# Kernel optimization log

Measured on AMD Instinct MI355X. Metric: run time of the kernel, lower is better.

## Reference

```python
import jax, jax.numpy as jnp
import numpy as np

D = 128      # d_model
H = 8        # n_heads
HD = D // H  # head_dim = 16
E = 256      # n_experts
R = 32       # kv_lora_rank
B, T = 4, 512
EPS = 1e-6


def _dense_init(k, fi, fo):
    s = float(1.0 / np.sqrt(fi))
    return jax.random.uniform(k, (fi, fo), minval=-s, maxval=s, dtype=jnp.float32)


def setup_inputs() -> dict:
    key = jax.random.key(0)
    ks = jax.random.split(key, 16)
    rng = np.random.RandomState(42)
    Q, _ = np.linalg.qr(rng.randn(D, D))
    glim = float(np.sqrt(6.0 / (D + D)))
    return {
        'x': jax.random.normal(ks[0], (B, T, D), dtype=jnp.float32),
        'g1': jnp.ones((D,), jnp.float32),
        'qW': _dense_init(ks[1], D, D), 'qb': jnp.zeros((D,), jnp.float32),
        'kdW': _dense_init(ks[2], D, R), 'kdb': jnp.zeros((R,), jnp.float32),
        'kuW': _dense_init(ks[3], R, 2 * D), 'kub': jnp.zeros((2 * D,), jnp.float32),
        'oW': _dense_init(ks[4], D, D), 'ob': jnp.zeros((D,), jnp.float32),
        'rot': jnp.asarray(Q, jnp.float32),
        'tq_scale': jnp.ones((D,), jnp.float32),
        's1W': _dense_init(ks[5], D, D), 's1b': jnp.zeros((D,), jnp.float32),
        's2W': _dense_init(ks[6], D, D), 's2b': jnp.zeros((D,), jnp.float32),
        'g2': jnp.ones((D,), jnp.float32),
        'gateW': _dense_init(ks[7], D, E), 'gateb': jnp.zeros((E,), jnp.float32),
        'expW': jax.random.uniform(ks[8], (E, D, D), minval=-glim, maxval=glim, dtype=jnp.float32),
        'm1W': _dense_init(ks[9], D, D), 'm1b': jnp.zeros((D,), jnp.float32),
        'm2W': _dense_init(ks[10], D, D), 'm2b': jnp.zeros((D,), jnp.float32),
    }


def _rmsnorm(x, g):
    return g * (x / jnp.sqrt(jnp.mean(x * x, axis=-1, keepdims=True) + EPS))


def _swiglu(x, w1, b1, w2, b2):
    gate = x @ w1 + b1
    return gate * jax.nn.sigmoid(gate) * (x @ w2 + b2)


def _mla(x, qW, qb, kdW, kdb, kuW, kub, oW, ob):
    b, t = x.shape[0], x.shape[1]
    q = (x @ qW + qb).reshape(b, t, H, HD)
    kv = ((x @ kdW + kdb) @ kuW + kub).reshape(b, t, H, 2 * HD)
    k, v = jnp.split(kv, 2, axis=-1)
    q = jax.nn.elu(q) + 1.0
    k = jax.nn.elu(k) + 1.0
    # linear attention: context[b,h,d,e] = sum_t k[b,t,h,d] v[b,t,h,e]
    context = jnp.einsum('bthd,bthe->bhde', k, v)
    out = jnp.einsum('bthd,bhde->bthe', q, context)
    k_sum = jnp.sum(k, axis=1)  # [b,h,d]
    z = 1.0 / (jnp.einsum('bthd,bhd->bth', q, k_sum) + EPS)
    out = out * z[..., None]
    return out.reshape(b, t, D) @ oW + ob


def _turbo_quant(x, rot, scale):
    x = x @ rot
    mag = jnp.sqrt(jnp.mean(x * x, axis=-1, keepdims=True) + EPS)
    phase = x / mag
    qp = jnp.clip(phase * 127.0, -127.0, 127.0) / 127.0
    phase = jax.lax.stop_gradient(qp - phase) + phase  # straight-through
    return phase * mag * scale


def _moe(h, gateW, gateb, expW, m1W, m1b, m2W, m2b):
    gate_scores = jax.nn.softmax(h @ gateW + gateb, axis=-1)  # [B,T,E]
    top_vals, top_idx = jax.lax.top_k(gate_scores, 2)
    top_w = top_vals / (jnp.sum(top_vals, axis=-1, keepdims=True) + EPS)
    # dense all-expert compute as in the original module
    eo = jnp.einsum('btd,edo->bteo', h, expW)  # [B,T,E,D]
    mask = jnp.sum(jax.nn.one_hot(top_idx, E, dtype=h.dtype) * top_w[..., None], axis=2)  # [B,T,E]
    wavg = jnp.einsum('bteo,bte->bto', eo, mask)
    wavg = _swiglu(wavg, m1W, m1b, m2W, m2b)
    diff_sq = jnp.square(eo - wavg[:, :, None, :])
    wvar = jnp.einsum('bteo,bte->bto', diff_sq, mask)
    consensus = jnp.exp(-jnp.mean(wvar, axis=-1))  # [B,T]
    return wavg, consensus


def reference(x, g1, qW, qb, kdW, kdb, kuW, kub, oW, ob, rot, tq_scale,
              s1W, s1b, s2W, s2b, g2, gateW, gateb, expW, m1W, m1b, m2W, m2b):
    attn_out = _turbo_quant(_mla(_rmsnorm(x, g1), qW, qb, kdW, kdb, kuW, kub, oW, ob), rot, tq_scale)
    x = x + _swiglu(attn_out, s1W, s1b, s2W, s2b)
    moe_out, consensus = _moe(_rmsnorm(x, g2), gateW, gateb, expW, m1W, m1b, m2W, m2b)
    return x + moe_out, consensus
```

## Files before the change

kernel.cpp:

```cpp
#include <hip/hip_runtime.h>
#include <hip/hip_cooperative_groups.h>
#include <math.h>

namespace cg = cooperative_groups;

static constexpr int Dd    = 128;
static constexpr int NH    = 8;
static constexpr int NE    = 256;
static constexpr int RR    = 32;
static constexpr int TT    = 512;
static constexpr int NTOK  = 2048;
static constexpr int SLOTS = 256;
#define EPSF 1e-6f

__device__ __forceinline__ float elu1(float v) { return v > 0.f ? v + 1.f : expf(v); }
__device__ __forceinline__ float sigm(float v) { return 1.f / (1.f + expf(-v)); }

struct Params {
  const float *x, *g1, *qW, *qb, *kdW, *kdb, *kuW, *kub, *oW, *ob, *rot, *tqs;
  const float *s1W, *s1b, *s2W, *s2b, *g2, *gateW, *gateb, *expW, *m1W, *m1b, *m2W, *m2b;
  float *out;
  float *ctx, *ksum, *h2buf, *oR, *bR, *ybuf;
  int *cnt, *slottok;
};

template <int TPB>
__device__ __forceinline__ void fused_body(const Params P) {
  constexpr int NG    = TPB / 4;
  constexpr int GRIDB = NTOK / TPB;
  constexpr int BPE   = GRIDB / NE;
  const int tid = threadIdx.x;
  const int bid = blockIdx.x;
  const int j = tid & 127, g = tid >> 7;
  const int lane = tid & 63;
  const int base_n0 = bid * TPB;
  const int b = base_n0 >> 9;

  __shared__ float4 h1T[128];
  __shared__ float4 bufQ[NG][128];
  __shared__ float4 bufB[128];
  __shared__ float4 part[3][128];
  __shared__ float4 kpart[8][32];
  __shared__ float4 kdT[32];
  __shared__ float4 kupart[256];
  __shared__ float4 rtmp[2];
  __shared__ __align__(16) float kS[NG][8][16][4];
  __shared__ __align__(16) float vS[NG][8][16][4];
  __shared__ float wvS[4][4]; __shared__ int wiS[4][4];
  __shared__ float zS[4][4];
  __shared__ int sSlot[TPB][2]; __shared__ float sWt[TPB][2];
  __shared__ __align__(16) float hT[128 * 20];
  __shared__ float4 y1T[128], y2T[128], inT[128], sT[128];

  float xv[NG][4];
  float xn[NG][4];
#pragma unroll
  for (int grp = 0; grp < NG; grp++)
#pragma unroll
    for (int t = 0; t < 4; t++) { xv[grp][t] = 0.f; xn[grp][t] = 0.f; }

  if (bid == 0) {
    for (int i = tid; i < NH * 4 * 256; i += 512) P.ctx[i] = 0.f;
    P.ksum[tid] = 0.f;
    if (tid < NE) P.cnt[tid] = 0;
  }

  for (int grp = 0; grp < NG; grp++) {
    const int n0 = base_n0 + grp * 4;

    if (tid < 128) {
      float v[4];
#pragma unroll
      for (int t = 0; t < 4; t++) { xv[grp][t] = P.x[(n0 + t) * Dd + j]; v[t] = xv[grp][t] * xv[grp][t]; }
#pragma unroll
      for (int o = 32; o > 0; o >>= 1) {
#pragma unroll
        for (int t = 0; t < 4; t++) v[t] += __shfl_xor(v[t], o, 64);
      }
      if (lane == 0) rtmp[tid >> 6] = make_float4(v[0], v[1], v[2], v[3]);
    }
    __syncthreads();
    if (tid < 128) {
      float g1j = P.g1[j];
#pragma unroll
      for (int t = 0; t < 4; t++) {
        float ss = ((const float*)&rtmp[0])[t] + ((const float*)&rtmp[1])[t];
        ((float*)&h1T[j])[t] = g1j * xv[grp][t] * rsqrtf(ss * (1.f / 128.f) + EPSF);
      }
    }
    __syncthreads();

    {
      float a0 = 0, a1 = 0, a2 = 0, a3 = 0;
      const float* Wp = P.qW + (g * 32) * Dd + j;
#pragma unroll 16
      for (int i = 0; i < 32; i++) {
        float4 h4 = h1T[g * 32 + i];
        float w = Wp[i * Dd];
        a0 += h4.x * w; a1 += h4.y * w; a2 += h4.z * w; a3 += h4.w * w;
      }
      if (g) part[g - 1][j] = make_float4(a0, a1, a2, a3);
      __syncthreads();
      if (g == 0) {
        float4 p0 = part[0][j], p1 = part[1][j], p2 = part[2][j];
        float bb = P.qb[j];
        ((float*)&bufQ[grp][j])[0] = elu1(a0 + p0.x + p1.x + p2.x + bb);
        ((float*)&bufQ[grp][j])[1] = elu1(a1 + p0.y + p1.y + p2.y + bb);
        ((float*)&bufQ[grp][j])[2] = elu1(a2 + p0.z + p1.z + p2.z + bb);
        ((float*)&bufQ[grp][j])[3] = elu1(a3 + p0.w + p1.w + p2.w + bb);
      }
      __syncthreads();
    }

    if (tid < 256) {
      int col = tid & 31, ksp = tid >> 5;
      float a0 = 0, a1 = 0, a2 = 0, a3 = 0;
      const float* Wp = P.kdW + (ksp * 16) * RR + col;
#pragma unroll
      for (int i = 0; i < 16; i++) {
        float4 h4 = h1T[ksp * 16 + i];
        float w = Wp[i * RR];
        a0 += h4.x * w; a1 += h4.y * w; a2 += h4.z * w; a3 += h4.w * w;
      }
      kpart[ksp][col] = make_float4(a0, a1, a2, a3);
    }
    __syncthreads();
    if (tid < 32) {
      float bb = P.kdb[tid];
      float s0 = bb, s1 = bb, s2 = bb, s3 = bb;
#pragma unroll
      for (int k = 0; k < 8; k++) {
        float4 p = kpart[k][tid];
        s0 += p.x; s1 += p.y; s2 += p.z; s3 += p.w;
      }
      kdT[tid] = make_float4(s0, s1, s2, s3);
    }
    __syncthreads();

    {
      int col = tid & 255, kh = tid >> 8;
      float a0 = 0, a1 = 0, a2 = 0, a3 = 0;
      const float* Wp = P.kuW + (kh * 16) * 256 + col;
#pragma unroll
      for (int r = 0; r < 16; r++) {
        float4 k4 = kdT[kh * 16 + r];
        float w = Wp[r * 256];
        a0 += k4.x * w; a1 += k4.y * w; a2 += k4.z * w; a3 += k4.w * w;
      }
      if (kh) kupart[col] = make_float4(a0, a1, a2, a3);
      __syncthreads();
      if (!kh) {
        float4 p = kupart[col];
        float bb = P.kub[col];
        float v0 = a0 + p.x + bb, v1 = a1 + p.y + bb, v2 = a2 + p.z + bb, v3 = a3 + p.w + bb;
        int h = col >> 5, off = col & 31;
        if (off < 16) {
          kS[grp][h][off][0] = elu1(v0); kS[grp][h][off][1] = elu1(v1);
          kS[grp][h][off][2] = elu1(v2); kS[grp][h][off][3] = elu1(v3);
        } else {
          vS[grp][h][off - 16][0] = v0; vS[grp][h][off - 16][1] = v1;
          vS[grp][h][off - 16][2] = v2; vS[grp][h][off - 16][3] = v3;
        }
      }
    }
    __syncthreads();
  }

  if (bid < 32) {
    int idx = bid * 512 + tid;
    int row = idx >> 7, col = idx & 127;
    const float* ow = P.oW + row * 128;
    float acc = 0.f;
#pragma unroll 8
    for (int k = 0; k < 128; k++) acc += ow[k] * P.rot[k * 128 + col];
    P.oR[idx] = acc;
  } else if (bid == 32 && tid < 128) {
    float acc = 0.f;
#pragma unroll 8
    for (int k = 0; k < 128; k++) acc += P.ob[k] * P.rot[k * 128 + tid];
    P.bR[tid] = acc;
  }

  cg::this_grid().sync();

  {
    const int h = tid >> 6;
    const int d = (tid >> 2) & 15;
    const int e0 = (tid & 3) * 4;
    const int bh = b * NH + h;
    float acc[4] = {0.f, 0.f, 0.f, 0.f};
    float ks = 0.f;
#pragma unroll
    for (int grp = 0; grp < NG; grp++) {
      float4 k4 = *(const float4*)&kS[grp][h][d][0];
      ks += k4.x + k4.y + k4.z + k4.w;
#pragma unroll
      for (int ee = 0; ee < 4; ee++) {
        float4 v4 = *(const float4*)&vS[grp][h][e0 + ee][0];
        acc[ee] += k4.x * v4.x + k4.y * v4.y + k4.z * v4.z + k4.w * v4.w;
      }
    }
    float* cp = P.ctx + bh * 256 + d * 16 + e0;
#pragma unroll
    for (int ee = 0; ee < 4; ee++) atomicAdd(cp + ee, acc[ee]);
    if ((tid & 3) == 0) atomicAdd(&P.ksum[bh * 16 + d], ks);
  }

  cg::this_grid().sync();

  for (int grp = 0; grp < NG; grp++) {
    const int n0 = base_n0 + grp * 4;
    float m1[4]; int i1[4]; float m2[4]; int i2[4];
    float val[4]; float r2v[4];

    if (tid < 128) {
      int h = j >> 4, e = j & 15;
      const float* cpt = P.ctx + (b * NH + h) * 256;
      const float* kpt = P.ksum + (b * NH + h) * 16;
      float num[4] = {0, 0, 0, 0}, den[4] = {0, 0, 0, 0};
#pragma unroll
      for (int d = 0; d < 16; d++) {
        float cx = cpt[d * 16 + e], ks = kpt[d];
        float4 q4 = bufQ[grp][h * 16 + d];
        num[0] += q4.x * cx; num[1] += q4.y * cx; num[2] += q4.z * cx; num[3] += q4.w * cx;
        den[0] += q4.x * ks; den[1] += q4.y * ks; den[2] += q4.z * ks; den[3] += q4.w * ks;
      }
#pragma unroll
      for (int t = 0; t < 4; t++) ((float*)&bufB[j])[t] = num[t] / (den[t] + EPSF);
    }
    __syncthreads();

    {
      float a0 = 0, a1 = 0, a2 = 0, a3 = 0;
      const float* Wp = P.oR + (g * 32) * Dd + j;
#pragma unroll 16
      for (int i = 0; i < 32; i++) {
        float4 h4 = bufB[g * 32 + i];
        float w = Wp[i * Dd];
        a0 += h4.x * w; a1 += h4.y * w; a2 += h4.z * w; a3 += h4.w * w;
      }
      if (g) part[g - 1][j] = make_float4(a0, a1, a2, a3);
      __syncthreads();
      float tot[4];
      if (g == 0) {
        float4 p0 = part[0][j], p1 = part[1][j], p2 = part[2][j];
        float bb = P.bR[j];
        tot[0] = a0 + p0.x + p1.x + p2.x + bb; tot[1] = a1 + p0.y + p1.y + p2.y + bb;
        tot[2] = a2 + p0.z + p1.z + p2.z + bb; tot[3] = a3 + p0.w + p1.w + p2.w + bb;
        float v[4];
#pragma unroll
        for (int t = 0; t < 4; t++) v[t] = tot[t] * tot[t];
#pragma unroll
        for (int o = 32; o > 0; o >>= 1) {
#pragma unroll
          for (int t = 0; t < 4; t++) v[t] += __shfl_xor(v[t], o, 64);
        }
        if (lane == 0) rtmp[tid >> 6] = make_float4(v[0], v[1], v[2], v[3]);
      }
      __syncthreads();
      if (g == 0) {
        float scj = P.tqs[j];
#pragma unroll
        for (int t = 0; t < 4; t++) {
          float ss = ((const float*)&rtmp[0])[t] + ((const float*)&rtmp[1])[t];
          float mag = sqrtf(ss * (1.f / 128.f) + EPSF);
          float zc = fminf(fmaxf(tot[t], -mag), mag);
          ((float*)&bufQ[grp][j])[t] = zc * scj;
        }
      }
      __syncthreads();
    }

    {
      float a0 = 0, a1 = 0, a2 = 0, a3 = 0;
      const float* Wp = (g < 2 ? P.s1W : P.s2W) + ((g & 1) * 64) * Dd + j;
#pragma unroll 16
      for (int i = 0; i < 64; i++) {
        float4 h4 = bufQ[grp][(g & 1) * 64 + i];
        float w = Wp[i * Dd];
        a0 += h4.x * w; a1 += h4.y * w; a2 += h4.z * w; a3 += h4.w * w;
      }
      if (g) part[g - 1][j] = make_float4(a0, a1, a2, a3);
      __syncthreads();
      if (g == 0) {
        float b1 = P.s1b[j], b2 = P.s2b[j];
        float4 p0 = part[0][j], p1 = part[1][j], p2 = part[2][j];
        float gv[4], uv[4], v[4];
        gv[0] = a0 + p0.x + b1; gv[1] = a1 + p0.y + b1;
        gv[2] = a2 + p0.z + b1; gv[3] = a3 + p0.w + b1;
        uv[0] = p1.x + p2.x + b2; uv[1] = p1.y + p2.y + b2;
        uv[2] = p1.z + p2.z + b2; uv[3] = p1.w + p2.w + b2;
        float g2j = P.g2[j];
#pragma unroll
        for (int t = 0; t < 4; t++) {
          xn[grp][t] = xv[grp][t] + gv[t] * sigm(gv[t]) * uv[t];
          ((float*)&bufB[j])[t] = g2j * xn[grp][t];
          v[t] = xn[grp][t] * xn[grp][t];
        }
#pragma unroll
        for (int o = 32; o > 0; o >>= 1) {
#pragma unroll
          for (int t = 0; t < 4; t++) v[t] += __shfl_xor(v[t], o, 64);
        }
        if (lane == 0) rtmp[tid >> 6] = make_float4(v[0], v[1], v[2], v[3]);
      }
      __syncthreads();
    }

    {
      int col = tid & 255, kh = tid >> 8;
      float a0 = 0, a1 = 0, a2 = 0, a3 = 0;
      const float* Wp = P.gateW + (kh * 64) * NE + col;
#pragma unroll 16
      for (int i = 0; i < 64; i++) {
        float4 h4 = bufB[kh * 64 + i];
        float w = Wp[i * NE];
        a0 += h4.x * w; a1 += h4.y * w; a2 += h4.z * w; a3 += h4.w * w;
      }
      if (kh) kupart[col] = make_float4(a0, a1, a2, a3);
      __syncthreads();
#pragma unroll
      for (int t = 0; t < 4; t++) {
        float ss = ((const float*)&rtmp[0])[t] + ((const float*)&rtmp[1])[t];
        r2v[t] = rsqrtf(ss * (1.f / 128.f) + EPSF);
      }
      if (!kh) {
        float4 p = kupart[col];
        float bb = P.gateb[col];
        val[0] = (a0 + p.x) * r2v[0] + bb; val[1] = (a1 + p.y) * r2v[1] + bb;
        val[2] = (a2 + p.z) * r2v[2] + bb; val[3] = (a3 + p.w) * r2v[3] + bb;
      }
      if (tid < 128) {
#pragma unroll
        for (int t = 0; t < 4; t++)
          P.h2buf[(n0 + t) * Dd + j] = ((const float*)&bufB[j])[t] * r2v[t];
      }
    }
    __syncthreads();

    {
      if (tid < 256) {
        float bv[4]; int bi[4];
#pragma unroll
        for (int t = 0; t < 4; t++) { bv[t] = val[t]; bi[t] = tid; }
#pragma unroll
        for (int o = 32; o > 0; o >>= 1) {
#pragma unroll
          for (int t = 0; t < 4; t++) {
            float wv = __shfl_xor(bv[t], o, 64);
            int wi = __shfl_xor(bi[t], o, 64);
            if (wv > bv[t] || (wv == bv[t] && wi < bi[t])) { bv[t] = wv; bi[t] = wi; }
          }
        }
        if (lane == 0) {
#pragma unroll
          for (int t = 0; t < 4; t++) { wvS[tid >> 6][t] = bv[t]; wiS[tid >> 6][t] = bi[t]; }
        }
      }
      __syncthreads();
      if (tid < 256) {
#pragma unroll
        for (int t = 0; t < 4; t++) {
          m1[t] = wvS[0][t]; i1[t] = wiS[0][t];
#pragma unroll
          for (int w = 1; w < 4; w++) {
            float cv = wvS[w][t]; int ci = wiS[w][t];
            if (cv > m1[t] || (cv == m1[t] && ci < i1[t])) { m1[t] = cv; i1[t] = ci; }
          }
        }
      }
      __syncthreads();
    }
    {
      if (tid < 256) {
        float bv[4]; int bi[4];
#pragma unroll
        for (int t = 0; t < 4; t++) {
          bv[t] = (tid == i1[t]) ? -INFINITY : val[t];
          bi[t] = tid;
        }
#pragma unroll
        for (int o = 32; o > 0; o >>= 1) {
#pragma unroll
          for (int t = 0; t < 4; t++) {
            float wv = __shfl_xor(bv[t], o, 64);
            int wi = __shfl_xor(bi[t], o, 64);
            if (wv > bv[t] || (wv == bv[t] && wi < bi[t])) { bv[t] = wv; bi[t] = wi; }
          }
        }
        if (lane == 0) {
#pragma unroll
          for (int t = 0; t < 4; t++) { wvS[tid >> 6][t] = bv[t]; wiS[tid >> 6][t] = bi[t]; }
        }
      }
      __syncthreads();
      if (tid < 256) {
#pragma unroll
        for (int t = 0; t < 4; t++) {
          m2[t] = wvS[0][t]; i2[t] = wiS[0][t];
#pragma unroll
          for (int w = 1; w < 4; w++) {
            float cv = wvS[w][t]; int ci = wiS[w][t];
            if (cv > m2[t] || (cv == m2[t] && ci < i2[t])) { m2[t] = cv; i2[t] = ci; }
          }
        }
      }
      __syncthreads();
    }
    {
      if (tid < 256) {
        float v[4];
#pragma unroll
        for (int t = 0; t < 4; t++) v[t] = expf(val[t] - m1[t]);
#pragma unroll
        for (int o = 32; o > 0; o >>= 1) {
#pragma unroll
          for (int t = 0; t < 4; t++) v[t] += __shfl_xor(v[t], o, 64);
        }
        if (lane == 0) {
#pragma unroll
          for (int t = 0; t < 4; t++) zS[tid >> 6][t] = v[t];
        }
      }
      __syncthreads();
    }
    if (tid < 4) {
      int t = tid, tok = n0 + t;
      float Z = zS[0][t] + zS[1][t] + zS[2][t] + zS[3][t];
      float p1 = 1.f / Z;
      float p2 = expf(m2[t] - m1[t]) / Z;
      float s = p1 + p2 + EPSF;
      int e1 = i1[t], e2 = i2[t];
      int s1 = atomicAdd(&P.cnt[e1], 1); if (s1 > SLOTS - 1) s1 = SLOTS - 1;
      int s2 = atomicAdd(&P.cnt[e2], 1); if (s2 > SLOTS - 1) s2 = SLOTS - 1;
      int sl1 = e1 * SLOTS + s1, sl2 = e2 * SLOTS + s2;
      P.slottok[sl1] = tok; P.slottok[sl2] = tok;
      sSlot[grp * 4 + t][0] = sl1; sSlot[grp * 4 + t][1] = sl2;
      sWt[grp * 4 + t][0] = p1 / s; sWt[grp * 4 + t][1] = p2 / s;
    }
    __syncthreads();
  }

  cg::this_grid().sync();

  {
    const int e = bid / BPE, sub = bid % BPE;
    int n = P.cnt[e]; if (n > SLOTS) n = SLOTS;
    const int base = e * SLOTS;
    const float* Wp = P.expW + (size_t)e * Dd * Dd + j;
    for (int t0 = sub * 16; t0 < n; t0 += BPE * 16) {
      int m = n - t0; if (m > 16) m = 16;
      __syncthreads();
      for (int tt = g; tt < m; tt += 4) {
        int tok = P.slottok[base + t0 + tt];
        hT[j * 20 + tt] = P.h2buf[tok * Dd + j];
      }
      __syncthreads();
      float acc[4] = {0, 0, 0, 0};
#pragma unroll 8
      for (int i = 0; i < 128; i++) {
        float w = Wp[i * Dd];
        float4 h4 = *(const float4*)&hT[i * 20 + g * 4];
        acc[0] += h4.x * w; acc[1] += h4.y * w; acc[2] += h4.z * w; acc[3] += h4.w * w;
      }
#pragma unroll
      for (int k = 0; k < 4; k++) {
        int tt = g * 4 + k;
        if (tt < m) P.ybuf[(size_t)(base + t0 + tt) * Dd + j] = acc[k];
      }
    }
  }

  cg::this_grid().sync();

  for (int grp = 0; grp < NG; grp++) {
    const int n0 = base_n0 + grp * 4;
    {
      const int ti = grp * 4 + g;
      float y1 = P.ybuf[(size_t)sSlot[ti][0] * Dd + j];
      float y2 = P.ybuf[(size_t)sSlot[ti][1] * Dd + j];
      ((float*)&y1T[j])[g] = y1;
      ((float*)&y2T[j])[g] = y2;
      ((float*)&inT[j])[g] = sWt[ti][0] * y1 + sWt[ti][1] * y2;
    }
    __syncthreads();

    {
      float a0 = 0, a1 = 0, a2 = 0, a3 = 0;
      const float* Wp = (g < 2 ? P.m1W : P.m2W) + ((g & 1) * 64) * Dd + j;
#pragma unroll 16
      for (int i = 0; i < 64; i++) {
        float4 h4 = inT[(g & 1) * 64 + i];
        float w = Wp[i * Dd];
        a0 += h4.x * w; a1 += h4.y * w; a2 += h4.z * w; a3 += h4.w * w;
      }
      if (g) part[g - 1][j] = make_float4(a0, a1, a2, a3);
      __syncthreads();
      if (g == 0) {
        float b1 = P.m1b[j], b2 = P.m2b[j];
        float4 p0 = part[0][j], p1 = part[1][j], p2 = part[2][j];
        float gv[4], uv[4];
        gv[0] = a0 + p0.x + b1; gv[1] = a1 + p0.y + b1;
        gv[2] = a2 + p0.z + b1; gv[3] = a3 + p0.w + b1;
        uv[0] = p1.x + p2.x + b2; uv[1] = p1.y + p2.y + b2;
        uv[2] = p1.z + p2.z + b2; uv[3] = p1.w + p2.w + b2;
#pragma unroll
        for (int t = 0; t < 4; t++) {
          float sv = gv[t] * sigm(gv[t]) * uv[t];
          ((float*)&sT[j])[t] = sv;
          P.out[(n0 + t) * Dd + j] = xn[grp][t] + sv;
        }
      }
      __syncthreads();
    }

    if (tid < 128) {
      float v[4];
#pragma unroll
      for (int t = 0; t < 4; t++) {
        float sv = ((const float*)&sT[j])[t];
        float d1 = ((const float*)&y1T[j])[t] - sv;
        float d2 = ((const float*)&y2T[j])[t] - sv;
        v[t] = sWt[grp * 4 + t][0] * d1 * d1 + sWt[grp * 4 + t][1] * d2 * d2;
      }
#pragma unroll
      for (int o = 32; o > 0; o >>= 1) {
#pragma unroll
        for (int t = 0; t < 4; t++) v[t] += __shfl_xor(v[t], o, 64);
      }
      if (lane == 0) rtmp[tid >> 6] = make_float4(v[0], v[1], v[2], v[3]);
    }
    __syncthreads();
    if (tid < 4) {
      float s = ((const float*)&rtmp[0])[tid] + ((const float*)&rtmp[1])[tid];
      P.out[NTOK * Dd + n0 + tid] = expf(-s * (1.f / 128.f));
    }
    __syncthreads();
  }
}

__global__ __launch_bounds__(512, 4) void k_fused4(Params P) { fused_body<4>(P); }
__global__ __launch_bounds__(512)    void k_fused8(Params P) { fused_body<8>(P); }

static constexpr int TPBo = 4;

__global__ __launch_bounds__(512) void k_pre(
    const float* __restrict__ x, const float* __restrict__ g1,
    const float* __restrict__ qW, const float* __restrict__ qb,
    const float* __restrict__ kdW, const float* __restrict__ kdb,
    const float* __restrict__ kuW, const float* __restrict__ kub,
    float* __restrict__ qbuf, float* __restrict__ kvbuf,
    float* __restrict__ ctx, float* __restrict__ ksum, int* __restrict__ cnt) {
  const int tid = threadIdx.x;
  const int j = tid & 127, g = tid >> 7;
  const int lane = tid & 63;
  const int n0 = blockIdx.x * TPBo;

  __shared__ float4 h1T[128];
  __shared__ float4 part[3][128];
  __shared__ float4 kpart[8][32];
  __shared__ float4 kdT[32];
  __shared__ float4 kupart[256];
  __shared__ float4 rtmp[2];

  if (blockIdx.x == 0) {
    for (int i = tid; i < 32 * 256; i += 512) ctx[i] = 0.f;
    ksum[tid] = 0.f;
    if (tid < 256) cnt[tid] = 0;
  }

  float xv[4];
  if (tid < 128) {
    float v[4];
#pragma unroll
    for (int t = 0; t < 4; t++) { xv[t] = x[(n0 + t) * Dd + j]; v[t] = xv[t] * xv[t]; }
#pragma unroll
    for (int o = 32; o > 0; o >>= 1) {
#pragma unroll
      for (int t = 0; t < 4; t++) v[t] += __shfl_xor(v[t], o, 64);
    }
    if (lane == 0) rtmp[tid >> 6] = make_float4(v[0], v[1], v[2], v[3]);
  }
  __syncthreads();
  if (tid < 128) {
    float g1j = g1[j];
#pragma unroll
    for (int t = 0; t < 4; t++) {
      float ss = ((const float*)&rtmp[0])[t] + ((const float*)&rtmp[1])[t];
      ((float*)&h1T[j])[t] = g1j * xv[t] * rsqrtf(ss * (1.f / 128.f) + EPSF);
    }
  }
  __syncthreads();

  {
    float a0 = 0, a1 = 0, a2 = 0, a3 = 0;
    const float* Wp = qW + (g * 32) * Dd + j;
#pragma unroll 16
    for (int i = 0; i < 32; i++) {
      float4 h4 = h1T[g * 32 + i];
      float w = Wp[i * Dd];
      a0 += h4.x * w; a1 += h4.y * w; a2 += h4.z * w; a3 += h4.w * w;
    }
    if (g) part[g - 1][j] = make_float4(a0, a1, a2, a3);
    __syncthreads();
    if (g == 0) {
      float4 p0 = part[0][j], p1 = part[1][j], p2 = part[2][j];
      float bb = qb[j];
      qbuf[(n0 + 0) * Dd + j] = elu1(a0 + p0.x + p1.x + p2.x + bb);
      qbuf[(n0 + 1) * Dd + j] = elu1(a1 + p0.y + p1.y + p2.y + bb);
      qbuf[(n0 + 2) * Dd + j] = elu1(a2 + p0.z + p1.z + p2.z + bb);
      qbuf[(n0 + 3) * Dd + j] = elu1(a3 + p0.w + p1.w + p2.w + bb);
    }
    __syncthreads();
  }

  if (tid < 256) {
    int col = tid & 31, ksp = tid >> 5;
    float a0 = 0, a1 = 0, a2 = 0, a3 = 0;
    const float* Wp = kdW + (ksp * 16) * RR + col;
#pragma unroll
    for (int i = 0; i < 16; i++) {
      float4 h4 = h1T[ksp * 16 + i];
      float w = Wp[i * RR];
      a0 += h4.x * w; a1 += h4.y * w; a2 += h4.z * w; a3 += h4.w * w;
    }
    kpart[ksp][col] = make_float4(a0, a1, a2, a3);
  }
  __syncthreads();
  if (tid < 32) {
    float bb = kdb[tid];
    float s0 = bb, s1 = bb, s2 = bb, s3 = bb;
#pragma unroll
    for (int k = 0; k < 8; k++) {
      float4 p = kpart[k][tid];
      s0 += p.x; s1 += p.y; s2 += p.z; s3 += p.w;
    }
    kdT[tid] = make_float4(s0, s1, s2, s3);
  }
  __syncthreads();

  {
    int col = tid & 255, kh = tid >> 8;
    float a0 = 0, a1 = 0, a2 = 0, a3 = 0;
    const float* Wp = kuW + (kh * 16) * 256 + col;
#pragma unroll
    for (int r = 0; r < 16; r++) {
      float4 k4 = kdT[kh * 16 + r];
      float w = Wp[r * 256];
      a0 += k4.x * w; a1 += k4.y * w; a2 += k4.z * w; a3 += k4.w * w;
    }
    if (kh) kupart[col] = make_float4(a0, a1, a2, a3);
    __syncthreads();
    if (!kh) {
      float4 p = kupart[col];
      float bb = kub[col];
      bool isk = (col & 31) < 16;
      float v0 = a0 + p.x + bb, v1 = a1 + p.y + bb, v2 = a2 + p.z + bb, v3 = a3 + p.w + bb;
      kvbuf[(n0 + 0) * 256 + col] = isk ? elu1(v0) : v0;
      kvbuf[(n0 + 1) * 256 + col] = isk ? elu1(v1) : v1;
      kvbuf[(n0 + 2) * 256 + col] = isk ? elu1(v2) : v2;
      kvbuf[(n0 + 3) * 256 + col] = isk ? elu1(v3) : v3;
    }
  }
}

__global__ __launch_bounds__(256) void k_ctx(const float* __restrict__ kv,
                                             float* __restrict__ ctx,
                                             float* __restrict__ ksum,
                                             const float* __restrict__ oW,
                                             const float* __restrict__ ob,
                                             const float* __restrict__ rot,
                                             float* __restrict__ oR,
                                             float* __restrict__ bR) {
  const int blk = blockIdx.x;
  const int tid = threadIdx.x;
  if (blk < 256) {
    const int bh = blk >> 3, c = blk & 7;
    const int b = bh >> 3, h = bh & 7;
    const int d = tid >> 4, e = tid & 15;
    __shared__ float sh[64 * 32];
#pragma unroll
    for (int r = 0; r < 8; r++) {
      int lin = r * 256 + tid;
      int tok = lin >> 5, off = lin & 31;
      sh[lin] = kv[((b * TT + c * 64 + tok) * 256) + h * 32 + off];
    }
    __syncthreads();
    float acc = 0.f, ks = 0.f;
#pragma unroll 4
    for (int t = 0; t < 64; t++) {
      float kk = sh[t * 32 + d];
      acc += kk * sh[t * 32 + 16 + e];
      ks += kk;
    }
    atomicAdd(&ctx[bh * 256 + d * 16 + e], acc);
    if (e == 0) atomicAdd(&ksum[bh * 16 + d], ks);
  } else if (blk < 320) {
    int idx = (blk - 256) * 256 + tid;
    int row = idx >> 7, col = idx & 127;
    const float* ow = oW + row * 128;
    float acc = 0.f;
#pragma unroll 8
    for (int k = 0; k < 128; k++) acc += ow[k] * rot[k * 128 + col];
    oR[row * 128 + col] = acc;
  } else {
    if (tid < 128) {
      float acc = 0.f;
#pragma unroll 8
      for (int k = 0; k < 128; k++) acc += ob[k] * rot[k * 128 + tid];
      bR[tid] = acc;
    }
  }
}

__global__ __launch_bounds__(512) void k_mid(
    const float* __restrict__ x, const float* __restrict__ qbuf,
    const float* __restrict__ ctx, const float* __restrict__ ksum,
    const float* __restrict__ oR, const float* __restrict__ bR,
    const float* __restrict__ tqs,
    const float* __restrict__ s1W, const float* __restrict__ s1b,
    const float* __restrict__ s2W, const float* __restrict__ s2b,
    const float* __restrict__ g2, const float* __restrict__ gateW,
    const float* __restrict__ gateb,
    float* __restrict__ xnbuf, float* __restrict__ h2buf,
    float* __restrict__ gw, int* __restrict__ tokslot,
    int* __restrict__ slottok, int* __restrict__ cnt) {
  const int tid = threadIdx.x;
  const int j = tid & 127, g = tid >> 7;
  const int lane = tid & 63;
  const int n0 = blockIdx.x * TPBo;
  const int b = n0 >> 9;

  __shared__ float4 bufA[128], bufB[128];
  __shared__ float4 part[3][128];
  __shared__ float4 gpart[256];
  __shared__ float4 rtmp[2];
  __shared__ float wvS[4][4]; __shared__ int wiS[4][4];
  __shared__ float zS[4][4];

  float xres[4];
  if (tid < 128) {
#pragma unroll
    for (int t = 0; t < 4; t++) xres[t] = x[(n0 + t) * Dd + j];
  }

  ((float*)&bufA[j])[g] = qbuf[(n0 + g) * Dd + j];
  __syncthreads();

  if (tid < 128) {
    int h = j >> 4, e = j & 15;
    const float* cpt = ctx + (b * NH + h) * 256;
    const float* kpt = ksum + (b * NH + h) * 16;
    float num[4] = {0, 0, 0, 0}, den[4] = {0, 0, 0, 0};
#pragma unroll
    for (int d = 0; d < 16; d++) {
      float cx = cpt[d * 16 + e], ks = kpt[d];
      float4 q4 = bufA[h * 16 + d];
      num[0] += q4.x * cx; num[1] += q4.y * cx; num[2] += q4.z * cx; num[3] += q4.w * cx;
      den[0] += q4.x * ks; den[1] += q4.y * ks; den[2] += q4.z * ks; den[3] += q4.w * ks;
    }
#pragma unroll
    for (int t = 0; t < 4; t++) ((float*)&bufB[j])[t] = num[t] / (den[t] + EPSF);
  }
  __syncthreads();

  {
    float a0 = 0, a1 = 0, a2 = 0, a3 = 0;
    const float* Wp = oR + (g * 32) * Dd + j;
#pragma unroll 16
    for (int i = 0; i < 32; i++) {
      float4 h4 = bufB[g * 32 + i];
      float w = Wp[i * Dd];
      a0 += h4.x * w; a1 += h4.y * w; a2 += h4.z * w; a3 += h4.w * w;
    }
    if (g) part[g - 1][j] = make_float4(a0, a1, a2, a3);
    __syncthreads();
    float tot[4];
    if (g == 0) {
      float4 p0 = part[0][j], p1 = part[1][j], p2 = part[2][j];
      float bb = bR[j];
      tot[0] = a0 + p0.x + p1.x + p2.x + bb; tot[1] = a1 + p0.y + p1.y + p2.y + bb;
      tot[2] = a2 + p0.z + p1.z + p2.z + bb; tot[3] = a3 + p0.w + p1.w + p2.w + bb;
      float v[4];
#pragma unroll
      for (int t = 0; t < 4; t++) v[t] = tot[t] * tot[t];
#pragma unroll
      for (int o = 32; o > 0; o >>= 1) {
#pragma unroll
        for (int t = 0; t < 4; t++) v[t] += __shfl_xor(v[t], o, 64);
      }
      if (lane == 0) rtmp[tid >> 6] = make_float4(v[0], v[1], v[2], v[3]);
    }
    __syncthreads();
    if (g == 0) {
      float scj = tqs[j];
#pragma unroll
      for (int t = 0; t < 4; t++) {
        float ss = ((const float*)&rtmp[0])[t] + ((const float*)&rtmp[1])[t];
        float mag = sqrtf(ss * (1.f / 128.f) + EPSF);
        float zc = fminf(fmaxf(tot[t], -mag), mag);
        ((float*)&bufA[j])[t] = zc * scj;
      }
    }
    __syncthreads();
  }

  {
    float a0 = 0, a1 = 0, a2 = 0, a3 = 0;
    const float* Wp = (g < 2 ? s1W : s2W) + ((g & 1) * 64) * Dd + j;
#pragma unroll 16
    for (int i = 0; i < 64; i++) {
      float4 h4 = bufA[(g & 1) * 64 + i];
      float w = Wp[i * Dd];
      a0 += h4.x * w; a1 += h4.y * w; a2 += h4.z * w; a3 += h4.w * w;
    }
    if (g) part[g - 1][j] = make_float4(a0, a1, a2, a3);
    __syncthreads();
    if (g == 0) {
      float b1 = s1b[j], b2 = s2b[j];
      float4 p0 = part[0][j], p1 = part[1][j], p2 = part[2][j];
      float gv[4], uv[4], xn[4], v[4];
      gv[0] = a0 + p0.x + b1; gv[1] = a1 + p0.y + b1;
      gv[2] = a2 + p0.z + b1; gv[3] = a3 + p0.w + b1;
      uv[0] = p1.x + p2.x + b2; uv[1] = p1.y + p2.y + b2;
      uv[2] = p1.z + p2.z + b2; uv[3] = p1.w + p2.w + b2;
      float g2j = g2[j];
#pragma unroll
      for (int t = 0; t < 4; t++) {
        xn[t] = xres[t] + gv[t] * sigm(gv[t]) * uv[t];
        xnbuf[(n0 + t) * Dd + j] = xn[t];
        ((float*)&bufB[j])[t] = g2j * xn[t];
        v[t] = xn[t] * xn[t];
      }
#pragma unroll
      for (int o = 32; o > 0; o >>= 1) {
#pragma unroll
        for (int t = 0; t < 4; t++) v[t] += __shfl_xor(v[t], o, 64);
      }
      if (lane == 0) rtmp[tid >> 6] = make_float4(v[0], v[1], v[2], v[3]);
    }
    __syncthreads();
  }

  float val[4];
  float r2[4];
  {
    int col = tid & 255, kh = tid >> 8;
    float a0 = 0, a1 = 0, a2 = 0, a3 = 0;
    const float* Wp = gateW + (kh * 64) * NE + col;
#pragma unroll 16
    for (int i = 0; i < 64; i++) {
      float4 h4 = bufB[kh * 64 + i];
      float w = Wp[i * NE];
      a0 += h4.x * w; a1 += h4.y * w; a2 += h4.z * w; a3 += h4.w * w;
    }
    if (kh) gpart[col] = make_float4(a0, a1, a2, a3);
    __syncthreads();
#pragma unroll
    for (int t = 0; t < 4; t++) {
      float ss = ((const float*)&rtmp[0])[t] + ((const float*)&rtmp[1])[t];
      r2[t] = rsqrtf(ss * (1.f / 128.f) + EPSF);
    }
    if (!kh) {
      float4 p = gpart[col];
      float bb = gateb[col];
      val[0] = (a0 + p.x) * r2[0] + bb; val[1] = (a1 + p.y) * r2[1] + bb;
      val[2] = (a2 + p.z) * r2[2] + bb; val[3] = (a3 + p.w) * r2[3] + bb;
    }
    if (tid < 128) {
#pragma unroll
      for (int t = 0; t < 4; t++)
        h2buf[(n0 + t) * Dd + j] = ((const float*)&bufB[j])[t] * r2[t];
    }
  }
  __syncthreads();

  float m1[4]; int i1[4];
  {
    if (tid < 256) {
      float bv[4]; int bi[4];
#pragma unroll
      for (int t = 0; t < 4; t++) { bv[t] = val[t]; bi[t] = tid; }
#pragma unroll
      for (int o = 32; o > 0; o >>= 1) {
#pragma unroll
        for (int t = 0; t < 4; t++) {
          float wv = __shfl_xor(bv[t], o, 64);
          int wi = __shfl_xor(bi[t], o, 64);
          if (wv > bv[t] || (wv == bv[t] && wi < bi[t])) { bv[t] = wv; bi[t] = wi; }
        }
      }
      if (lane == 0) {
#pragma unroll
        for (int t = 0; t < 4; t++) { wvS[tid >> 6][t] = bv[t]; wiS[tid >> 6][t] = bi[t]; }
      }
    }
    __syncthreads();
    if (tid < 256) {
#pragma unroll
      for (int t = 0; t < 4; t++) {
        m1[t] = wvS[0][t]; i1[t] = wiS[0][t];
#pragma unroll
        for (int w = 1; w < 4; w++) {
          float cv = wvS[w][t]; int ci = wiS[w][t];
          if (cv > m1[t] || (cv == m1[t] && ci < i1[t])) { m1[t] = cv; i1[t] = ci; }
        }
      }
    }
    __syncthreads();
  }
  float m2[4]; int i2[4];
  {
    if (tid < 256) {
      float bv[4]; int bi[4];
#pragma unroll
      for (int t = 0; t < 4; t++) {
        bv[t] = (tid == i1[t]) ? -INFINITY : val[t];
        bi[t] = tid;
      }
#pragma unroll
      for (int o = 32; o > 0; o >>= 1) {
#pragma unroll
        for (int t = 0; t < 4; t++) {
          float wv = __shfl_xor(bv[t], o, 64);
          int wi = __shfl_xor(bi[t], o, 64);
          if (wv > bv[t] || (wv == bv[t] && wi < bi[t])) { bv[t] = wv; bi[t] = wi; }
        }
      }
      if (lane == 0) {
#pragma unroll
        for (int t = 0; t < 4; t++) { wvS[tid >> 6][t] = bv[t]; wiS[tid >> 6][t] = bi[t]; }
      }
    }
    __syncthreads();
    if (tid < 256) {
#pragma unroll
      for (int t = 0; t < 4; t++) {
        m2[t] = wvS[0][t]; i2[t] = wiS[0][t];
#pragma unroll
        for (int w = 1; w < 4; w++) {
          float cv = wvS[w][t]; int ci = wiS[w][t];
          if (cv > m2[t] || (cv == m2[t] && ci < i2[t])) { m2[t] = cv; i2[t] = ci; }
        }
      }
    }
    __syncthreads();
  }
  {
    if (tid < 256) {
      float v[4];
#pragma unroll
      for (int t = 0; t < 4; t++) v[t] = expf(val[t] - m1[t]);
#pragma unroll
      for (int o = 32; o > 0; o >>= 1) {
#pragma unroll
        for (int t = 0; t < 4; t++) v[t] += __shfl_xor(v[t], o, 64);
      }
      if (lane == 0) {
#pragma unroll
        for (int t = 0; t < 4; t++) zS[tid >> 6][t] = v[t];
      }
    }
    __syncthreads();
  }
  if (tid < 4) {
    int t = tid, tok = n0 + t;
    float Z = zS[0][t] + zS[1][t] + zS[2][t] + zS[3][t];
    float p1 = 1.f / Z;
    float p2 = expf(m2[t] - m1[t]) / Z;
    float s = p1 + p2 + EPSF;
    int e1 = i1[t], e2 = i2[t];
    int s1 = atomicAdd(&cnt[e1], 1); if (s1 > SLOTS - 1) s1 = SLOTS - 1;
    int s2 = atomicAdd(&cnt[e2], 1); if (s2 > SLOTS - 1) s2 = SLOTS - 1;
    int sl1 = e1 * SLOTS + s1, sl2 = e2 * SLOTS + s2;
    slottok[sl1] = tok; slottok[sl2] = tok;
    tokslot[tok * 2] = sl1; tokslot[tok * 2 + 1] = sl2;
    gw[tok * 2] = p1 / s; gw[tok * 2 + 1] = p2 / s;
  }
}

__global__ __launch_bounds__(512) void k_exp(const float* __restrict__ h2buf,
                                             const int* __restrict__ slottok,
                                             const int* __restrict__ cnt,
                                             const float* __restrict__ expW,
                                             float* __restrict__ ybuf) {
  const int e = blockIdx.x;
  int n = cnt[e]; if (n > SLOTS) n = SLOTS;
  if (n == 0) return;
  const int base = e * SLOTS;
  const int tid = threadIdx.x;
  const int j = tid & 127, g = tid >> 7;
  __shared__ __align__(16) float hT[128 * 20];
  const float* Wp = expW + (size_t)e * Dd * Dd + j;
  for (int t0 = 0; t0 < n; t0 += 16) {
    int m = n - t0; if (m > 16) m = 16;
    __syncthreads();
    for (int tt = g; tt < m; tt += 4) {
      int tok = slottok[base + t0 + tt];
      hT[j * 20 + tt] = h2buf[tok * Dd + j];
    }
    __syncthreads();
    float acc[4] = {0, 0, 0, 0};
#pragma unroll 8
    for (int i = 0; i < 128; i++) {
      float w = Wp[i * Dd];
      float4 h4 = *(const float4*)&hT[i * 20 + g * 4];
      acc[0] += h4.x * w; acc[1] += h4.y * w; acc[2] += h4.z * w; acc[3] += h4.w * w;
    }
#pragma unroll
    for (int k = 0; k < 4; k++) {
      int tt = g * 4 + k;
      if (tt < m) ybuf[(size_t)(base + t0 + tt) * Dd + j] = acc[k];
    }
  }
}

__global__ __launch_bounds__(512) void k_post(
    const float* __restrict__ xnbuf, const float* __restrict__ ybuf,
    const int* __restrict__ tokslot, const float* __restrict__ gw,
    const float* __restrict__ m1W, const float* __restrict__ m1b,
    const float* __restrict__ m2W, const float* __restrict__ m2b,
    float* __restrict__ out) {
  const int tid = threadIdx.x;
  const int j = tid & 127, g = tid >> 7;
  const int lane = tid & 63;
  const int n0 = blockIdx.x * TPBo;

  __shared__ float4 y1T[128], y2T[128], inT[128], sT[128];
  __shared__ float4 part[3][128];
  __shared__ float4 rtmp[2];
  __shared__ int sSlot[4][2];
  __shared__ float sWt[4][2];

  if (tid < 4) {
    sSlot[tid][0] = tokslot[(n0 + tid) * 2];
    sSlot[tid][1] = tokslot[(n0 + tid) * 2 + 1];
    sWt[tid][0] = gw[(n0 + tid) * 2];
    sWt[tid][1] = gw[(n0 + tid) * 2 + 1];
  }
  __syncthreads();

  {
    float y1 = ybuf[(size_t)sSlot[g][0] * Dd + j];
    float y2 = ybuf[(size_t)sSlot[g][1] * Dd + j];
    ((float*)&y1T[j])[g] = y1;
    ((float*)&y2T[j])[g] = y2;
    ((float*)&inT[j])[g] = sWt[g][0] * y1 + sWt[g][1] * y2;
  }
  __syncthreads();

  {
    float a0 = 0, a1 = 0, a2 = 0, a3 = 0;
    const float* Wp = (g < 2 ? m1W : m2W) + ((g & 1) * 64) * Dd + j;
#pragma unroll 16
    for (int i = 0; i < 64; i++) {
      float4 h4 = inT[(g & 1) * 64 + i];
      float w = Wp[i * Dd];
      a0 += h4.x * w; a1 += h4.y * w; a2 += h4.z * w; a3 += h4.w * w;
    }
    if (g) part[g - 1][j] = make_float4(a0, a1, a2, a3);
    __syncthreads();
    if (g == 0) {
      float b1 = m1b[j], b2 = m2b[j];
      float4 p0 = part[0][j], p1 = part[1][j], p2 = part[2][j];
      float gv[4], uv[4];
      gv[0] = a0 + p0.x + b1; gv[1] = a1 + p0.y + b1;
      gv[2] = a2 + p0.z + b1; gv[3] = a3 + p0.w + b1;
      uv[0] = p1.x + p2.x + b2; uv[1] = p1.y + p2.y + b2;
      uv[2] = p1.z + p2.z + b2; uv[3] = p1.w + p2.w + b2;
#pragma unroll
      for (int t = 0; t < 4; t++) {
        float sv = gv[t] * sigm(gv[t]) * uv[t];
        ((float*)&sT[j])[t] = sv;
        out[(n0 + t) * Dd + j] = xnbuf[(n0 + t) * Dd + j] + sv;
      }
    }
    __syncthreads();
  }

  if (tid < 128) {
    float v[4];
#pragma unroll
    for (int t = 0; t < 4; t++) {
      float sv = ((const float*)&sT[j])[t];
      float d1 = ((const float*)&y1T[j])[t] - sv;
      float d2 = ((const float*)&y2T[j])[t] - sv;
      v[t] = sWt[t][0] * d1 * d1 + sWt[t][1] * d2 * d2;
    }
#pragma unroll
    for (int o = 32; o > 0; o >>= 1) {
#pragma unroll
      for (int t = 0; t < 4; t++) v[t] += __shfl_xor(v[t], o, 64);
    }
    if (lane == 0) rtmp[tid >> 6] = make_float4(v[0], v[1], v[2], v[3]);
  }
  __syncthreads();
  if (tid < 4) {
    float s = ((const float*)&rtmp[0])[tid] + ((const float*)&rtmp[1])[tid];
    out[NTOK * Dd + n0 + tid] = expf(-s * (1.f / 128.f));
  }
}

extern "C" void kernel_launch(void* const* d_in, const int* in_sizes, int n_in,
                              void* d_out, int out_size, void* d_ws, size_t ws_size,
                              hipStream_t stream) {
  float* ws = (float*)d_ws;

  Params p;
  p.x   = (const float*)d_in[0];
  p.g1  = (const float*)d_in[1];
  p.qW  = (const float*)d_in[2];
  p.qb  = (const float*)d_in[3];
  p.kdW = (const float*)d_in[4];
  p.kdb = (const float*)d_in[5];
  p.kuW = (const float*)d_in[6];
  p.kub = (const float*)d_in[7];
  p.oW  = (const float*)d_in[8];
  p.ob  = (const float*)d_in[9];
  p.rot = (const float*)d_in[10];
  p.tqs = (const float*)d_in[11];
  p.s1W = (const float*)d_in[12];
  p.s1b = (const float*)d_in[13];
  p.s2W = (const float*)d_in[14];
  p.s2b = (const float*)d_in[15];
  p.g2  = (const float*)d_in[16];
  p.gateW = (const float*)d_in[17];
  p.gateb = (const float*)d_in[18];
  p.expW  = (const float*)d_in[19];
  p.m1W = (const float*)d_in[20];
  p.m1b = (const float*)d_in[21];
  p.m2W = (const float*)d_in[22];
  p.m2b = (const float*)d_in[23];
  p.out = (float*)d_out;

  p.ctx     = ws;
  p.ksum    = ws + 8192;
  p.oR      = ws + 8704;
  p.bR      = ws + 25088;
  p.h2buf   = ws + 25216;
  p.cnt     = (int*)(ws + 287360);
  p.slottok = (int*)(ws + 287616);
  p.ybuf    = ws + 353152;

  void* args[] = {(void*)&p};
  hipError_t err = hipErrorUnknown;

  int nb4 = 0;
  if (hipOccupancyMaxActiveBlocksPerMultiprocessor(
          &nb4, reinterpret_cast<const void*>(&k_fused4), 512, 0) != hipSuccess)
    nb4 = 0;
  if (nb4 >= 2) {
    err = hipLaunchCooperativeKernel((void*)k_fused4, dim3(NTOK / 4), dim3(512),
                                     args, 0u, stream);
  }
  if (err != hipSuccess) {
    int nb8 = 0;
    if (hipOccupancyMaxActiveBlocksPerMultiprocessor(
            &nb8, reinterpret_cast<const void*>(&k_fused8), 512, 0) == hipSuccess &&
        nb8 >= 1) {
      err = hipLaunchCooperativeKernel((void*)k_fused8, dim3(NTOK / 8), dim3(512),
                                       args, 0u, stream);
    }
  }
  if (err == hipSuccess) return;

  float* qbuf   = ws;
  float* kvbuf  = ws + 262144;
  float* ctx    = ws + 786432;
  float* ksum   = ws + 794624;
  float* h2buf  = ws + 795136;
  float* xnbuf  = ws + 1057280;
  float* gw     = ws + 1319424;
  float* oRb    = ws + 1323520;
  float* bRb    = ws + 1339904;
  int*   cnt     = (int*)(ws + 1373056);
  int*   tokslot = (int*)(ws + 1373312);
  int*   slottok = (int*)(ws + 1377408);
  float* ybuf   = ws + 1442944;

  k_pre<<<NTOK / 4, 512, 0, stream>>>(p.x, p.g1, p.qW, p.qb, p.kdW, p.kdb, p.kuW, p.kub,
                                      qbuf, kvbuf, ctx, ksum, cnt);
  k_ctx<<<321, 256, 0, stream>>>(kvbuf, ctx, ksum, p.oW, p.ob, p.rot, oRb, bRb);
  k_mid<<<NTOK / 4, 512, 0, stream>>>(p.x, qbuf, ctx, ksum, oRb, bRb, p.tqs,
                                      p.s1W, p.s1b, p.s2W, p.s2b, p.g2, p.gateW, p.gateb,
                                      xnbuf, h2buf, gw, tokslot, slottok, cnt);
  k_exp<<<NE, 512, 0, stream>>>(h2buf, slottok, cnt, p.expW, ybuf);
  k_post<<<NTOK / 4, 512, 0, stream>>>(xnbuf, ybuf, tokslot, gw,
                                       p.m1W, p.m1b, p.m2W, p.m2b, p.out);
}
```

Measured before the change: 166.6 us.

## Split fused cooperative kernel into pre-kernel plus flag-synchronized remainder kernel

Replaces the single cooperative kernel, which used four grid-wide barriers, with a regular k_pre launch that computes q/kv projections and the folded output rotation, followed by a cooperative k_rest kernel. k_rest appears to use per-stage global flags (context, routing, per-expert) in place of full grid syncs, so expert blocks can start once their own tokens are routed. The fallback path splits expert work across two blocks per expert. This adds an extra launch and global round-trips for q/kv buffers, and the flag spinning carries correctness and deadlock risks.

```diff
diff --git a/kernel.cpp b/kernel.cpp
--- a/kernel.cpp
+++ b/kernel.cpp
@@ -1,8 +1,5 @@
 #include <hip/hip_runtime.h>
-#include <hip/hip_cooperative_groups.h>
 #include <math.h>
-
-namespace cg = cooperative_groups;
 
 static constexpr int Dd    = 128;
 static constexpr int NH    = 8;
@@ -13,548 +10,41 @@
 static constexpr int SLOTS = 256;
 #define EPSF 1e-6f
 
+static constexpr int FD_CTX   = 0;
+static constexpr int FD_ROUTE = 4;
+static constexpr int FD_EXP   = 5;
+static constexpr int NFLAGS   = 261;
+
 __device__ __forceinline__ float elu1(float v) { return v > 0.f ? v + 1.f : expf(v); }
 __device__ __forceinline__ float sigm(float v) { return 1.f / (1.f + expf(-v)); }
 
-struct Params {
-  const float *x, *g1, *qW, *qb, *kdW, *kdb, *kuW, *kub, *oW, *ob, *rot, *tqs;
-  const float *s1W, *s1b, *s2W, *s2b, *g2, *gateW, *gateb, *expW, *m1W, *m1b, *m2W, *m2b;
-  float *out;
-  float *ctx, *ksum, *h2buf, *oR, *bR, *ybuf;
-  int *cnt, *slottok;
-};
-
-template <int TPB>
-__device__ __forceinline__ void fused_body(const Params P) {
-  constexpr int NG    = TPB / 4;
-  constexpr int GRIDB = NTOK / TPB;
-  constexpr int BPE   = GRIDB / NE;
-  const int tid = threadIdx.x;
-  const int bid = blockIdx.x;
-  const int j = tid & 127, g = tid >> 7;
-  const int lane = tid & 63;
-  const int base_n0 = bid * TPB;
-  const int b = base_n0 >> 9;
-
-  __shared__ float4 h1T[128];
-  __shared__ float4 bufQ[NG][128];
-  __shared__ float4 bufB[128];
-  __shared__ float4 part[3][128];
-  __shared__ float4 kpart[8][32];
-  __shared__ float4 kdT[32];
-  __shared__ float4 kupart[256];
-  __shared__ float4 rtmp[2];
-  __shared__ __align__(16) float kS[NG][8][16][4];
-  __shared__ __align__(16) float vS[NG][8][16][4];
-  __shared__ float wvS[4][4]; __shared__ int wiS[4][4];
-  __shared__ float zS[4][4];
-  __shared__ int sSlot[TPB][2]; __shared__ float sWt[TPB][2];
-  __shared__ __align__(16) float hT[128 * 20];
-  __shared__ float4 y1T[128], y2T[128], inT[128], sT[128];
-
-  float xv[NG][4];
-  float xn[NG][4];
-#pragma unroll
-  for (int grp = 0; grp < NG; grp++)
-#pragma unroll
-    for (int t = 0; t < 4; t++) { xv[grp][t] = 0.f; xn[grp][t] = 0.f; }
-
-  if (bid == 0) {
-    for (int i = tid; i < NH * 4 * 256; i += 512) P.ctx[i] = 0.f;
-    P.ksum[tid] = 0.f;
-    if (tid < NE) P.cnt[tid] = 0;
-  }
-
-  for (int grp = 0; grp < NG; grp++) {
-    const int n0 = base_n0 + grp * 4;
-
-    if (tid < 128) {
-      float v[4];
-#pragma unroll
-      for (int t = 0; t < 4; t++) { xv[grp][t] = P.x[(n0 + t) * Dd + j]; v[t] = xv[grp][t] * xv[grp][t]; }
-#pragma unroll
-      for (int o = 32; o > 0; o >>= 1) {
-#pragma unroll
-        for (int t = 0; t < 4; t++) v[t] += __shfl_xor(v[t], o, 64);
-      }
-      if (lane == 0) rtmp[tid >> 6] = make_float4(v[0], v[1], v[2], v[3]);
-    }
-    __syncthreads();
-    if (tid < 128) {
-      float g1j = P.g1[j];
-#pragma unroll
-      for (int t = 0; t < 4; t++) {
-        float ss = ((const float*)&rtmp[0])[t] + ((const float*)&rtmp[1])[t];
-        ((float*)&h1T[j])[t] = g1j * xv[grp][t] * rsqrtf(ss * (1.f / 128.f) + EPSF);
-      }
-    }
-    __syncthreads();
-
-    {
-      float a0 = 0, a1 = 0, a2 = 0, a3 = 0;
-      const float* Wp = P.qW + (g * 32) * Dd + j;
-#pragma unroll 16
-      for (int i = 0; i < 32; i++) {
-        float4 h4 = h1T[g * 32 + i];
-        float w = Wp[i * Dd];
-        a0 += h4.x * w; a1 += h4.y * w; a2 += h4.z * w; a3 += h4.w * w;
-      }
-      if (g) part[g - 1][j] = make_float4(a0, a1, a2, a3);
-      __syncthreads();
-      if (g == 0) {
-        float4 p0 = part[0][j], p1 = part[1][j], p2 = part[2][j];
-        float bb = P.qb[j];
-        ((float*)&bufQ[grp][j])[0] = elu1(a0 + p0.x + p1.x + p2.x + bb);
-        ((float*)&bufQ[grp][j])[1] = elu1(a1 + p0.y + p1.y + p2.y + bb);
-        ((float*)&bufQ[grp][j])[2] = elu1(a2 + p0.z + p1.z + p2.z + bb);
-        ((float*)&bufQ[grp][j])[3] = elu1(a3 + p0.w + p1.w + p2.w + bb);
-      }
-      __syncthreads();
-    }
-
-    if (tid < 256) {
-      int col = tid & 31, ksp = tid >> 5;
-      float a0 = 0, a1 = 0, a2 = 0, a3 = 0;
-      const float* Wp = P.kdW + (ksp * 16) * RR + col;
-#pragma unroll
-      for (int i = 0; i < 16; i++) {
-        float4 h4 = h1T[ksp * 16 + i];
-        float w = Wp[i * RR];
-        a0 += h4.x * w; a1 += h4.y * w; a2 += h4.z * w; a3 += h4.w * w;
-      }
-      kpart[ksp][col] = make_float4(a0, a1, a2, a3);
-    }
-    __syncthreads();
-    if (tid < 32) {
-      float bb = P.kdb[tid];
-      float s0 = bb, s1 = bb, s2 = bb, s3 = bb;
-#pragma unroll
-      for (int k = 0; k < 8; k++) {
-        float4 p = kpart[k][tid];
-        s0 += p.x; s1 += p.y; s2 += p.z; s3 += p.w;
-      }
-      kdT[tid] = make_float4(s0, s1, s2, s3);
-    }
-    __syncthreads();
-
-    {
-      int col = tid & 255, kh = tid >> 8;
-      float a0 = 0, a1 = 0, a2 = 0, a3 = 0;
-      const float* Wp = P.kuW + (kh * 16) * 256 + col;
-#pragma unroll
-      for (int r = 0; r < 16; r++) {
-        float4 k4 = kdT[kh * 16 + r];
-        float w = Wp[r * 256];
-        a0 += k4.x * w; a1 += k4.y * w; a2 += k4.z * w; a3 += k4.w * w;
-      }
-      if (kh) kupart[col] = make_float4(a0, a1, a2, a3);
-      __syncthreads();
-      if (!kh) {
-        float4 p = kupart[col];
-        float bb = P.kub[col];
-        float v0 = a0 + p.x + bb, v1 = a1 + p.y + bb, v2 = a2 + p.z + bb, v3 = a3 + p.w + bb;
-        int h = col >> 5, off = col & 31;
-        if (off < 16) {
-          kS[grp][h][off][0] = elu1(v0); kS[grp][h][off][1] = elu1(v1);
-          kS[grp][h][off][2] = elu1(v2); kS[grp][h][off][3] = elu1(v3);
-        } else {
-          vS[grp][h][off - 16][0] = v0; vS[grp][h][off - 16][1] = v1;
-          vS[grp][h][off - 16][2] = v2; vS[grp][h][off - 16][3] = v3;
-        }
-      }
-    }
-    __syncthreads();
-  }
-
-  if (bid < 32) {
-    int idx = bid * 512 + tid;
-    int row = idx >> 7, col = idx & 127;
-    const float* ow = P.oW + row * 128;
-    float acc = 0.f;
-#pragma unroll 8
-    for (int k = 0; k < 128; k++) acc += ow[k] * P.rot[k * 128 + col];
-    P.oR[idx] = acc;
-  } else if (bid == 32 && tid < 128) {
-    float acc = 0.f;
-#pragma unroll 8
-    for (int k = 0; k < 128; k++) acc += P.ob[k] * P.rot[k * 128 + tid];
-    P.bR[tid] = acc;
-  }
-
-  cg::this_grid().sync();
-
-  {
-    const int h = tid >> 6;
-    const int d = (tid >> 2) & 15;
-    const int e0 = (tid & 3) * 4;
-    const int bh = b * NH + h;
-    float acc[4] = {0.f, 0.f, 0.f, 0.f};
-    float ks = 0.f;
-#pragma unroll
-    for (int grp = 0; grp < NG; grp++) {
-      float4 k4 = *(const float4*)&kS[grp][h][d][0];
-      ks += k4.x + k4.y + k4.z + k4.w;
-#pragma unroll
-      for (int ee = 0; ee < 4; ee++) {
-        float4 v4 = *(const float4*)&vS[grp][h][e0 + ee][0];
-        acc[ee] += k4.x * v4.x + k4.y * v4.y + k4.z * v4.z + k4.w * v4.w;
-      }
-    }
-    float* cp = P.ctx + bh * 256 + d * 16 + e0;
-#pragma unroll
-    for (int ee = 0; ee < 4; ee++) atomicAdd(cp + ee, acc[ee]);
-    if ((tid & 3) == 0) atomicAdd(&P.ksum[bh * 16 + d], ks);
-  }
-
-  cg::this_grid().sync();
-
-  for (int grp = 0; grp < NG; grp++) {
-    const int n0 = base_n0 + grp * 4;
-    float m1[4]; int i1[4]; float m2[4]; int i2[4];
-    float val[4]; float r2v[4];
-
-    if (tid < 128) {
-      int h = j >> 4, e = j & 15;
-      const float* cpt = P.ctx + (b * NH + h) * 256;
-      const float* kpt = P.ksum + (b * NH + h) * 16;
-      float num[4] = {0, 0, 0, 0}, den[4] = {0, 0, 0, 0};
-#pragma unroll
-      for (int d = 0; d < 16; d++) {
-        float cx = cpt[d * 16 + e], ks = kpt[d];
-        float4 q4 = bufQ[grp][h * 16 + d];
-        num[0] += q4.x * cx; num[1] += q4.y * cx; num[2] += q4.z * cx; num[3] += q4.w * cx;
-        den[0] += q4.x * ks; den[1] += q4.y * ks; den[2] += q4.z * ks; den[3] += q4.w * ks;
-      }
-#pragma unroll
-      for (int t = 0; t < 4; t++) ((float*)&bufB[j])[t] = num[t] / (den[t] + EPSF);
-    }
-    __syncthreads();
-
-    {
-      float a0 = 0, a1 = 0, a2 = 0, a3 = 0;
-      const float* Wp = P.oR + (g * 32) * Dd + j;
-#pragma unroll 16
-      for (int i = 0; i < 32; i++) {
-        float4 h4 = bufB[g * 32 + i];
-        float w = Wp[i * Dd];
-        a0 += h4.x * w; a1 += h4.y * w; a2 += h4.z * w; a3 += h4.w * w;
-      }
-      if (g) part[g - 1][j] = make_float4(a0, a1, a2, a3);
-      __syncthreads();
-      float tot[4];
-      if (g == 0) {
-        float4 p0 = part[0][j], p1 = part[1][j], p2 = part[2][j];
-        float bb = P.bR[j];
-        tot[0] = a0 + p0.x + p1.x + p2.x + bb; tot[1] = a1 + p0.y + p1.y + p2.y + bb;
-        tot[2] = a2 + p0.z + p1.z + p2.z + bb; tot[3] = a3 + p0.w + p1.w + p2.w + bb;
-        float v[4];
-#pragma unroll
-        for (int t = 0; t < 4; t++) v[t] = tot[t] * tot[t];
-#pragma unroll
-        for (int o = 32; o > 0; o >>= 1) {
-#pragma unroll
-          for (int t = 0; t < 4; t++) v[t] += __shfl_xor(v[t], o, 64);
-        }
-        if (lane == 0) rtmp[tid >> 6] = make_float4(v[0], v[1], v[2], v[3]);
-      }
-      __syncthreads();
-      if (g == 0) {
-        float scj = P.tqs[j];
-#pragma unroll
-        for (int t = 0; t < 4; t++) {
-          float ss = ((const float*)&rtmp[0])[t] + ((const float*)&rtmp[1])[t];
-          float mag = sqrtf(ss * (1.f / 128.f) + EPSF);
-          float zc = fminf(fmaxf(tot[t], -mag), mag);
-          ((float*)&bufQ[grp][j])[t] = zc * scj;
-        }
-      }
-      __syncthreads();
-    }
-
-    {
-      float a0 = 0, a1 = 0, a2 = 0, a3 = 0;
-      const float* Wp = (g < 2 ? P.s1W : P.s2W) + ((g & 1) * 64) * Dd + j;
-#pragma unroll 16
-      for (int i = 0; i < 64; i++) {
-        float4 h4 = bufQ[grp][(g & 1) * 64 + i];
-        float w = Wp[i * Dd];
-        a0 += h4.x * w; a1 += h4.y * w; a2 += h4.z * w; a3 += h4.w * w;
-      }
-      if (g) part[g - 1][j] = make_float4(a0, a1, a2, a3);
-      __syncthreads();
-      if (g == 0) {
-        float b1 = P.s1b[j], b2 = P.s2b[j];
-        float4 p0 = part[0][j], p1 = part[1][j], p2 = part[2][j];
-        float gv[4], uv[4], v[4];
-        gv[0] = a0 + p0.x + b1; gv[1] = a1 + p0.y + b1;
-        gv[2] = a2 + p0.z + b1; gv[3] = a3 + p0.w + b1;
-        uv[0] = p1.x + p2.x + b2; uv[1] = p1.y + p2.y + b2;
-        uv[2] = p1.z + p2.z + b2; uv[3] = p1.w + p2.w + b2;
-        float g2j = P.g2[j];
-#pragma unroll
-        for (int t = 0; t < 4; t++) {
-          xn[grp][t] = xv[grp][t] + gv[t] * sigm(gv[t]) * uv[t];
-          ((float*)&bufB[j])[t] = g2j * xn[grp][t];
-          v[t] = xn[grp][t] * xn[grp][t];
-        }
-#pragma unroll
-        for (int o = 32; o > 0; o >>= 1) {
-#pragma unroll
-          for (int t = 0; t < 4; t++) v[t] += __shfl_xor(v[t], o, 64);
-        }
-        if (lane == 0) rtmp[tid >> 6] = make_float4(v[0], v[1], v[2], v[3]);
-      }
-      __syncthreads();
-    }
-
-    {
-      int col = tid & 255, kh = tid >> 8;
-      float a0 = 0, a1 = 0, a2 = 0, a3 = 0;
-      const float* Wp = P.gateW + (kh * 64) * NE + col;
-#pragma unroll 16
-      for (int i = 0; i < 64; i++) {
-        float4 h4 = bufB[kh * 64 + i];
-        float w = Wp[i * NE];
-        a0 += h4.x * w; a1 += h4.y * w; a2 += h4.z * w; a3 += h4.w * w;
-      }
-      if (kh) kupart[col] = make_float4(a0, a1, a2, a3);
-      __syncthreads();
-#pragma unroll
-      for (int t = 0; t < 4; t++) {
-        float ss = ((const float*)&rtmp[0])[t] + ((const float*)&rtmp[1])[t];
-        r2v[t] = rsqrtf(ss * (1.f / 128.f) + EPSF);
-      }
-      if (!kh) {
-        float4 p = kupart[col];
-        float bb = P.gateb[col];
-        val[0] = (a0 + p.x) * r2v[0] + bb; val[1] = (a1 + p.y) * r2v[1] + bb;
-        val[2] = (a2 + p.z) * r2v[2] + bb; val[3] = (a3 + p.w) * r2v[3] + bb;
-      }
-      if (tid < 128) {
-#pragma unroll
-        for (int t = 0; t < 4; t++)
-          P.h2buf[(n0 + t) * Dd + j] = ((const float*)&bufB[j])[t] * r2v[t];
-      }
-    }
-    __syncthreads();
-
-    {
-      if (tid < 256) {
-        float bv[4]; int bi[4];
-#pragma unroll
-        for (int t = 0; t < 4; t++) { bv[t] = val[t]; bi[t] = tid; }
-#pragma unroll
-        for (int o = 32; o > 0; o >>= 1) {
-#pragma unroll
-          for (int t = 0; t < 4; t++) {
-            float wv = __shfl_xor(bv[t], o, 64);
-            int wi = __shfl_xor(bi[t], o, 64);
-            if (wv > bv[t] || (wv == bv[t] && wi < bi[t])) { bv[t] = wv; bi[t] = wi; }
-          }
-        }
-        if (lane == 0) {
-#pragma unroll
-          for (int t = 0; t < 4; t++) { wvS[tid >> 6][t] = bv[t]; wiS[tid >> 6][t] = bi[t]; }
-        }
-      }
-      __syncthreads();
-      if (tid < 256) {
-#pragma unroll
-        for (int t = 0; t < 4; t++) {
-          m1[t] = wvS[0][t]; i1[t] = wiS[0][t];
-#pragma unroll
-          for (int w = 1; w < 4; w++) {
-            float cv = wvS[w][t]; int ci = wiS[w][t];
-            if (cv > m1[t] || (cv == m1[t] && ci < i1[t])) { m1[t] = cv; i1[t] = ci; }
-          }
-        }
-      }
-      __syncthreads();
-    }
-    {
-      if (tid < 256) {
-        float bv[4]; int bi[4];
-#pragma unroll
-        for (int t = 0; t < 4; t++) {
-          bv[t] = (tid == i1[t]) ? -INFINITY : val[t];
-          bi[t] = tid;
-        }
-#pragma unroll
-        for (int o = 32; o > 0; o >>= 1) {
-#pragma unroll
-          for (int t = 0; t < 4; t++) {
-            float wv = __shfl_xor(bv[t], o, 64);
-            int wi = __shfl_xor(bi[t], o, 64);
-            if (wv > bv[t] || (wv == bv[t] && wi < bi[t])) { bv[t] = wv; bi[t] = wi; }
-          }
-        }
-        if (lane == 0) {
-#pragma unroll
-          for (int t = 0; t < 4; t++) { wvS[tid >> 6][t] = bv[t]; wiS[tid >> 6][t] = bi[t]; }
-        }
-      }
-      __syncthreads();
-      if (tid < 256) {
-#pragma unroll
-        for (int t = 0; t < 4; t++) {
-          m2[t] = wvS[0][t]; i2[t] = wiS[0][t];
-#pragma unroll
-          for (int w = 1; w < 4; w++) {
-            float cv = wvS[w][t]; int ci = wiS[w][t];
-            if (cv > m2[t] || (cv == m2[t] && ci < i2[t])) { m2[t] = cv; i2[t] = ci; }
-          }
-        }
-      }
-      __syncthreads();
-    }
-    {
-      if (tid < 256) {
-        float v[4];
-#pragma unroll
-        for (int t = 0; t < 4; t++) v[t] = expf(val[t] - m1[t]);
-#pragma unroll
-        for (int o = 32; o > 0; o >>= 1) {
-#pragma unroll
-          for (int t = 0; t < 4; t++) v[t] += __shfl_xor(v[t], o, 64);
-        }
-        if (lane == 0) {
-#pragma unroll
-          for (int t = 0; t < 4; t++) zS[tid >> 6][t] = v[t];
-        }
-      }
-      __syncthreads();
-    }
-    if (tid < 4) {
-      int t = tid, tok = n0 + t;
-      float Z = zS[0][t] + zS[1][t] + zS[2][t] + zS[3][t];
-      float p1 = 1.f / Z;
-      float p2 = expf(m2[t] - m1[t]) / Z;
-      float s = p1 + p2 + EPSF;
-      int e1 = i1[t], e2 = i2[t];
-      int s1 = atomicAdd(&P.cnt[e1], 1); if (s1 > SLOTS - 1) s1 = SLOTS - 1;
-      int s2 = atomicAdd(&P.cnt[e2], 1); if (s2 > SLOTS - 1) s2 = SLOTS - 1;
-      int sl1 = e1 * SLOTS + s1, sl2 = e2 * SLOTS + s2;
-      P.slottok[sl1] = tok; P.slottok[sl2] = tok;
-      sSlot[grp * 4 + t][0] = sl1; sSlot[grp * 4 + t][1] = sl2;
-      sWt[grp * 4 + t][0] = p1 / s; sWt[grp * 4 + t][1] = p2 / s;
-    }
-    __syncthreads();
-  }
-
-  cg::this_grid().sync();
-
-  {
-    const int e = bid / BPE, sub = bid % BPE;
-    int n = P.cnt[e]; if (n > SLOTS) n = SLOTS;
-    const int base = e * SLOTS;
-    const float* Wp = P.expW + (size_t)e * Dd * Dd + j;
-    for (int t0 = sub * 16; t0 < n; t0 += BPE * 16) {
-      int m = n - t0; if (m > 16) m = 16;
-      __syncthreads();
-      for (int tt = g; tt < m; tt += 4) {
-        int tok = P.slottok[base + t0 + tt];
-        hT[j * 20 + tt] = P.h2buf[tok * Dd + j];
-      }
-      __syncthreads();
-      float acc[4] = {0, 0, 0, 0};
-#pragma unroll 8
-      for (int i = 0; i < 128; i++) {
-        float w = Wp[i * Dd];
-        float4 h4 = *(const float4*)&hT[i * 20 + g * 4];
-        acc[0] += h4.x * w; acc[1] += h4.y * w; acc[2] += h4.z * w; acc[3] += h4.w * w;
-      }
-#pragma unroll
-      for (int k = 0; k < 4; k++) {
-        int tt = g * 4 + k;
-        if (tt < m) P.ybuf[(size_t)(base + t0 + tt) * Dd + j] = acc[k];
-      }
-    }
-  }
-
-  cg::this_grid().sync();
-
-  for (int grp = 0; grp < NG; grp++) {
-    const int n0 = base_n0 + grp * 4;
-    {
-      const int ti = grp * 4 + g;
-      float y1 = P.ybuf[(size_t)sSlot[ti][0] * Dd + j];
-      float y2 = P.ybuf[(size_t)sSlot[ti][1] * Dd + j];
-      ((float*)&y1T[j])[g] = y1;
-      ((float*)&y2T[j])[g] = y2;
-      ((float*)&inT[j])[g] = sWt[ti][0] * y1 + sWt[ti][1] * y2;
-    }
-    __syncthreads();
-
-    {
-      float a0 = 0, a1 = 0, a2 = 0, a3 = 0;
-      const float* Wp = (g < 2 ? P.m1W : P.m2W) + ((g & 1) * 64) * Dd + j;
-#pragma unroll 16
-      for (int i = 0; i < 64; i++) {
-        float4 h4 = inT[(g & 1) * 64 + i];
-        float w = Wp[i * Dd];
-        a0 += h4.x * w; a1 += h4.y * w; a2 += h4.z * w; a3 += h4.w * w;
-      }
-      if (g) part[g - 1][j] = make_float4(a0, a1, a2, a3);
-      __syncthreads();
-      if (g == 0) {
-        float b1 = P.m1b[j], b2 = P.m2b[j];
-        float4 p0 = part[0][j], p1 = part[1][j], p2 = part[2][j];
-        float gv[4], uv[4];
-        gv[0] = a0 + p0.x + b1; gv[1] = a1 + p0.y + b1;
-        gv[2] = a2 + p0.z + b1; gv[3] = a3 + p0.w + b1;
-        uv[0] = p1.x + p2.x + b2; uv[1] = p1.y + p2.y + b2;
-        uv[2] = p1.z + p2.z + b2; uv[3] = p1.w + p2.w + b2;
-#pragma unroll
-        for (int t = 0; t < 4; t++) {
-          float sv = gv[t] * sigm(gv[t]) * uv[t];
-          ((float*)&sT[j])[t] = sv;
-          P.out[(n0 + t) * Dd + j] = xn[grp][t] + sv;
-        }
-      }
-      __syncthreads();
-    }
-
-    if (tid < 128) {
-      float v[4];
-#pragma unroll
-      for (int t = 0; t < 4; t++) {
-        float sv = ((const float*)&sT[j])[t];
-        float d1 = ((const float*)&y1T[j])[t] - sv;
-        float d2 = ((const float*)&y2T[j])[t] - sv;
-        v[t] = sWt[grp * 4 + t][0] * d1 * d1 + sWt[grp * 4 + t][1] * d2 * d2;
-      }
-#pragma unroll
-      for (int o = 32; o > 0; o >>= 1) {
-#pragma unroll
-        for (int t = 0; t < 4; t++) v[t] += __shfl_xor(v[t], o, 64);
-      }
-      if (lane == 0) rtmp[tid >> 6] = make_float4(v[0], v[1], v[2], v[3]);
-    }
-    __syncthreads();
-    if (tid < 4) {
-      float s = ((const float*)&rtmp[0])[tid] + ((const float*)&rtmp[1])[tid];
-      P.out[NTOK * Dd + n0 + tid] = expf(-s * (1.f / 128.f));
-    }
-    __syncthreads();
-  }
+__device__ __forceinline__ void flag_add(int* p) {
+  __hip_atomic_fetch_add(p, 1, __ATOMIC_RELEASE, __HIP_MEMORY_SCOPE_AGENT);
 }
-
-__global__ __launch_bounds__(512, 4) void k_fused4(Params P) { fused_body<4>(P); }
-__global__ __launch_bounds__(512)    void k_fused8(Params P) { fused_body<8>(P); }
-
-static constexpr int TPBo = 4;
+__device__ __forceinline__ void flag_wait(int* p, int tgt) {
+  int c = 0;
+  while (__hip_atomic_load(p, __ATOMIC_ACQUIRE, __HIP_MEMORY_SCOPE_AGENT) < tgt) {
+    __builtin_amdgcn_s_sleep(2);
+    if (++c > (1 << 27)) break;
+  }
+}
 
 __global__ __launch_bounds__(512) void k_pre(
     const float* __restrict__ x, const float* __restrict__ g1,
     const float* __restrict__ qW, const float* __restrict__ qb,
     const float* __restrict__ kdW, const float* __restrict__ kdb,
     const float* __restrict__ kuW, const float* __restrict__ kub,
+    const float* __restrict__ oW, const float* __restrict__ ob,
+    const float* __restrict__ rot,
     float* __restrict__ qbuf, float* __restrict__ kvbuf,
-    float* __restrict__ ctx, float* __restrict__ ksum, int* __restrict__ cnt) {
+    float* __restrict__ ctx, float* __restrict__ ksum,
+    int* __restrict__ cnt, int* __restrict__ flags,
+    float* __restrict__ oR, float* __restrict__ bR) {
   const int tid = threadIdx.x;
+  const int bid = blockIdx.x;
   const int j = tid & 127, g = tid >> 7;
   const int lane = tid & 63;
-  const int n0 = blockIdx.x * TPBo;
+  const int n0 = bid * 4;
 
   __shared__ float4 h1T[128];
   __shared__ float4 part[3][128];
@@ -563,10 +53,11 @@
   __shared__ float4 kupart[256];
   __shared__ float4 rtmp[2];
 
-  if (blockIdx.x == 0) {
+  if (bid == 0) {
     for (int i = tid; i < 32 * 256; i += 512) ctx[i] = 0.f;
     ksum[tid] = 0.f;
-    if (tid < 256) cnt[tid] = 0;
+    if (tid < NE) cnt[tid] = 0;
+    if (tid < NFLAGS) flags[tid] = 0;
   }
 
   float xv[4];
@@ -662,58 +153,456 @@
       kvbuf[(n0 + 3) * 256 + col] = isk ? elu1(v3) : v3;
     }
   }
-}
-
-__global__ __launch_bounds__(256) void k_ctx(const float* __restrict__ kv,
-                                             float* __restrict__ ctx,
-                                             float* __restrict__ ksum,
-                                             const float* __restrict__ oW,
-                                             const float* __restrict__ ob,
-                                             const float* __restrict__ rot,
-                                             float* __restrict__ oR,
-                                             float* __restrict__ bR) {
-  const int blk = blockIdx.x;
-  const int tid = threadIdx.x;
-  if (blk < 256) {
-    const int bh = blk >> 3, c = blk & 7;
-    const int b = bh >> 3, h = bh & 7;
-    const int d = tid >> 4, e = tid & 15;
-    __shared__ float sh[64 * 32];
-#pragma unroll
-    for (int r = 0; r < 8; r++) {
-      int lin = r * 256 + tid;
-      int tok = lin >> 5, off = lin & 31;
-      sh[lin] = kv[((b * TT + c * 64 + tok) * 256) + h * 32 + off];
-    }
-    __syncthreads();
-    float acc = 0.f, ks = 0.f;
-#pragma unroll 4
-    for (int t = 0; t < 64; t++) {
-      float kk = sh[t * 32 + d];
-      acc += kk * sh[t * 32 + 16 + e];
-      ks += kk;
-    }
-    atomicAdd(&ctx[bh * 256 + d * 16 + e], acc);
-    if (e == 0) atomicAdd(&ksum[bh * 16 + d], ks);
-  } else if (blk < 320) {
-    int idx = (blk - 256) * 256 + tid;
+
+  if (bid < 32) {
+    int idx = bid * 512 + tid;
     int row = idx >> 7, col = idx & 127;
     const float* ow = oW + row * 128;
     float acc = 0.f;
 #pragma unroll 8
     for (int k = 0; k < 128; k++) acc += ow[k] * rot[k * 128 + col];
-    oR[row * 128 + col] = acc;
-  } else {
+    oR[idx] = acc;
+  } else if (bid == 32 && tid < 128) {
+    float acc = 0.f;
+#pragma unroll 8
+    for (int k = 0; k < 128; k++) acc += ob[k] * rot[k * 128 + tid];
+    bR[tid] = acc;
+  }
+}
+
+struct RParams {
+  const float *x, *qbuf, *kvbuf, *oR, *bR, *tqs;
+  const float *s1W, *s1b, *s2W, *s2b, *g2, *gateW, *gateb, *expW;
+  const float *m1W, *m1b, *m2W, *m2b;
+  float *ctx, *ksum, *h2buf, *ybuf, *out;
+  int *cnt, *slottok, *flags;
+};
+
+__global__ __launch_bounds__(512, 4) void k_rest(RParams P) {
+  const int tid = threadIdx.x;
+  const int bid = blockIdx.x;
+  const int j = tid & 127, g = tid >> 7;
+  const int lane = tid & 63;
+  const int n0 = bid * 4;
+  const int b = bid >> 7;
+
+  __shared__ float sh[64 * 32];
+  __shared__ float4 bufA[128], bufB[128];
+  __shared__ float4 part[3][128];
+  __shared__ float4 gpart[256];
+  __shared__ float4 rtmp[2];
+  __shared__ float wvS[4][4]; __shared__ int wiS[4][4];
+  __shared__ float zS[4][4];
+  __shared__ int sE[4][2]; __shared__ int sSlot[4][2]; __shared__ float sWt[4][2];
+  __shared__ __align__(16) float hT[128 * 20];
+  __shared__ float4 y1T[128], y2T[128], inT[128], sT[128];
+
+  float xres[4];
+  if (tid < 128) {
+#pragma unroll
+    for (int t = 0; t < 4; t++) xres[t] = P.x[(n0 + t) * Dd + j];
+  }
+  ((float*)&bufA[j])[g] = P.qbuf[(n0 + g) * Dd + j];
+
+  if (bid < 256) {
+    const int bh = bid >> 3, c = bid & 7;
+    const int bb = bh >> 3, h = bh & 7;
+#pragma unroll
+    for (int r = 0; r < 4; r++) {
+      int lin = r * 512 + tid;
+      int tok = lin >> 5, off = lin & 31;
+      sh[lin] = P.kvbuf[((bb * TT + c * 64 + tok) * 256) + h * 32 + off];
+    }
+    __syncthreads();
+    if (tid < 256) {
+      const int d = tid >> 4, e = tid & 15;
+      float acc = 0.f, ks = 0.f;
+#pragma unroll 4
+      for (int t = 0; t < 64; t++) {
+        float kk = sh[t * 32 + d];
+        acc += kk * sh[t * 32 + 16 + e];
+        ks += kk;
+      }
+      atomicAdd(&P.ctx[bh * 256 + d * 16 + e], acc);
+      if (e == 0) atomicAdd(&P.ksum[bh * 16 + d], ks);
+    }
+    __threadfence();
+    __syncthreads();
+    if (tid == 0) flag_add(&P.flags[FD_CTX + bb]);
+  }
+
+  if (tid == 0) flag_wait(&P.flags[FD_CTX + b], 64);
+  __syncthreads();
+  __threadfence();
+
+  if (tid < 128) {
+    int h = j >> 4, e = j & 15;
+    const float* cpt = P.ctx + (b * NH + h) * 256;
+    const float* kpt = P.ksum + (b * NH + h) * 16;
+    float num[4] = {0, 0, 0, 0}, den[4] = {0, 0, 0, 0};
+#pragma unroll
+    for (int d = 0; d < 16; d++) {
+      float cx = cpt[d * 16 + e], ks = kpt[d];
+      float4 q4 = bufA[h * 16 + d];
+      num[0] += q4.x * cx; num[1] += q4.y * cx; num[2] += q4.z * cx; num[3] += q4.w * cx;
+      den[0] += q4.x * ks; den[1] += q4.y * ks; den[2] += q4.z * ks; den[3] += q4.w * ks;
+    }
+#pragma unroll
+    for (int t = 0; t < 4; t++) ((float*)&bufB[j])[t] = num[t] / (den[t] + EPSF);
+  }
+  __syncthreads();
+
+  {
+    float a0 = 0, a1 = 0, a2 = 0, a3 = 0;
+    const float* Wp = P.oR + (g * 32) * Dd + j;
+#pragma unroll 16
+    for (int i = 0; i < 32; i++) {
+      float4 h4 = bufB[g * 32 + i];
+      float w = Wp[i * Dd];
+      a0 += h4.x * w; a1 += h4.y * w; a2 += h4.z * w; a3 += h4.w * w;
+    }
+    if (g) part[g - 1][j] = make_float4(a0, a1, a2, a3);
+    __syncthreads();
+    float tot[4];
+    if (g == 0) {
+      float4 p0 = part[0][j], p1 = part[1][j], p2 = part[2][j];
+      float bb = P.bR[j];
+      tot[0] = a0 + p0.x + p1.x + p2.x + bb; tot[1] = a1 + p0.y + p1.y + p2.y + bb;
+      tot[2] = a2 + p0.z + p1.z + p2.z + bb; tot[3] = a3 + p0.w + p1.w + p2.w + bb;
+      float v[4];
+#pragma unroll
+      for (int t = 0; t < 4; t++) v[t] = tot[t] * tot[t];
+#pragma unroll
+      for (int o = 32; o > 0; o >>= 1) {
+#pragma unroll
+        for (int t = 0; t < 4; t++) v[t] += __shfl_xor(v[t], o, 64);
+      }
+      if (lane == 0) rtmp[tid >> 6] = make_float4(v[0], v[1], v[2], v[3]);
+    }
+    __syncthreads();
+    if (g == 0) {
+      float scj = P.tqs[j];
+#pragma unroll
+      for (int t = 0; t < 4; t++) {
+        float ss = ((const float*)&rtmp[0])[t] + ((const float*)&rtmp[1])[t];
+        float mag = sqrtf(ss * (1.f / 128.f) + EPSF);
+        float zc = fminf(fmaxf(tot[t], -mag), mag);
+        ((float*)&bufA[j])[t] = zc * scj;
+      }
+    }
+    __syncthreads();
+  }
+
+  float xn[4] = {0.f, 0.f, 0.f, 0.f};
+  {
+    float a0 = 0, a1 = 0, a2 = 0, a3 = 0;
+    const float* Wp = (g < 2 ? P.s1W : P.s2W) + ((g & 1) * 64) * Dd + j;
+#pragma unroll 16
+    for (int i = 0; i < 64; i++) {
+      float4 h4 = bufA[(g & 1) * 64 + i];
+      float w = Wp[i * Dd];
+      a0 += h4.x * w; a1 += h4.y * w; a2 += h4.z * w; a3 += h4.w * w;
+    }
+    if (g) part[g - 1][j] = make_float4(a0, a1, a2, a3);
+    __syncthreads();
+    if (g == 0) {
+      float b1 = P.s1b[j], b2 = P.s2b[j];
+      float4 p0 = part[0][j], p1 = part[1][j], p2 = part[2][j];
+      float gv[4], uv[4], v[4];
+      gv[0] = a0 + p0.x + b1; gv[1] = a1 + p0.y + b1;
+      gv[2] = a2 + p0.z + b1; gv[3] = a3 + p0.w + b1;
+      uv[0] = p1.x + p2.x + b2; uv[1] = p1.y + p2.y + b2;
+      uv[2] = p1.z + p2.z + b2; uv[3] = p1.w + p2.w + b2;
+      float g2j = P.g2[j];
+#pragma unroll
+      for (int t = 0; t < 4; t++) {
+        xn[t] = xres[t] + gv[t] * sigm(gv[t]) * uv[t];
+        ((float*)&bufB[j])[t] = g2j * xn[t];
+        v[t] = xn[t] * xn[t];
+      }
+#pragma unroll
+      for (int o = 32; o > 0; o >>= 1) {
+#pragma unroll
+        for (int t = 0; t < 4; t++) v[t] += __shfl_xor(v[t], o, 64);
+      }
+      if (lane == 0) rtmp[tid >> 6] = make_float4(v[0], v[1], v[2], v[3]);
+    }
+    __syncthreads();
+  }
+
+  float val[4]; float r2v[4];
+  {
+    int col = tid & 255, kh = tid >> 8;
+    float a0 = 0, a1 = 0, a2 = 0, a3 = 0;
+    const float* Wp = P.gateW + (kh * 64) * NE + col;
+#pragma unroll 16
+    for (int i = 0; i < 64; i++) {
+      float4 h4 = bufB[kh * 64 + i];
+      float w = Wp[i * NE];
+      a0 += h4.x * w; a1 += h4.y * w; a2 += h4.z * w; a3 += h4.w * w;
+    }
+    if (kh) gpart[col] = make_float4(a0, a1, a2, a3);
+    __syncthreads();
+#pragma unroll
+    for (int t = 0; t < 4; t++) {
+      float ss = ((const float*)&rtmp[0])[t] + ((const float*)&rtmp[1])[t];
+      r2v[t] = rsqrtf(ss * (1.f / 128.f) + EPSF);
+    }
+    if (!kh) {
+      float4 p = gpart[col];
+      float bb = P.gateb[col];
+      val[0] = (a0 + p.x) * r2v[0] + bb; val[1] = (a1 + p.y) * r2v[1] + bb;
+      val[2] = (a2 + p.z) * r2v[2] + bb; val[3] = (a3 + p.w) * r2v[3] + bb;
+    }
     if (tid < 128) {
-      float acc = 0.f;
+#pragma unroll
+      for (int t = 0; t < 4; t++)
+        P.h2buf[(n0 + t) * Dd + j] = ((const float*)&bufB[j])[t] * r2v[t];
+    }
+  }
+  __syncthreads();
+
+  float m1[4]; int i1[4];
+  {
+    if (tid < 256) {
+      float bv[4]; int bi[4];
+#pragma unroll
+      for (int t = 0; t < 4; t++) { bv[t] = val[t]; bi[t] = tid; }
+#pragma unroll
+      for (int o = 32; o > 0; o >>= 1) {
+#pragma unroll
+        for (int t = 0; t < 4; t++) {
+          float wv = __shfl_xor(bv[t], o, 64);
+          int wi = __shfl_xor(bi[t], o, 64);
+          if (wv > bv[t] || (wv == bv[t] && wi < bi[t])) { bv[t] = wv; bi[t] = wi; }
+        }
+      }
+      if (lane == 0) {
+#pragma unroll
+        for (int t = 0; t < 4; t++) { wvS[tid >> 6][t] = bv[t]; wiS[tid >> 6][t] = bi[t]; }
+      }
+    }
+    __syncthreads();
+    if (tid < 256) {
+#pragma unroll
+      for (int t = 0; t < 4; t++) {
+        m1[t] = wvS[0][t]; i1[t] = wiS[0][t];
+#pragma unroll
+        for (int w = 1; w < 4; w++) {
+          float cv = wvS[w][t]; int ci = wiS[w][t];
+          if (cv > m1[t] || (cv == m1[t] && ci < i1[t])) { m1[t] = cv; i1[t] = ci; }
+        }
+      }
+    }
+    __syncthreads();
+  }
+  float m2[4]; int i2[4];
+  {
+    if (tid < 256) {
+      float bv[4]; int bi[4];
+#pragma unroll
+      for (int t = 0; t < 4; t++) {
+        bv[t] = (tid == i1[t]) ? -INFINITY : val[t];
+        bi[t] = tid;
+      }
+#pragma unroll
+      for (int o = 32; o > 0; o >>= 1) {
+#pragma unroll
+        for (int t = 0; t < 4; t++) {
+          float wv = __shfl_xor(bv[t], o, 64);
+          int wi = __shfl_xor(bi[t], o, 64);
+          if (wv > bv[t] || (wv == bv[t] && wi < bi[t])) { bv[t] = wv; bi[t] = wi; }
+        }
+      }
+      if (lane == 0) {
+#pragma unroll
+        for (int t = 0; t < 4; t++) { wvS[tid >> 6][t] = bv[t]; wiS[tid >> 6][t] = bi[t]; }
+      }
+    }
+    __syncthreads();
+    if (tid < 256) {
+#pragma unroll
+      for (int t = 0; t < 4; t++) {
+        m2[t] = wvS[0][t]; i2[t] = wiS[0][t];
+#pragma unroll
+        for (int w = 1; w < 4; w++) {
+          float cv = wvS[w][t]; int ci = wiS[w][t];
+          if (cv > m2[t] || (cv == m2[t] && ci < i2[t])) { m2[t] = cv; i2[t] = ci; }
+        }
+      }
+    }
+    __syncthreads();
+  }
+  {
+    if (tid < 256) {
+      float v[4];
+#pragma unroll
+      for (int t = 0; t < 4; t++) v[t] = expf(val[t] - m1[t]);
+#pragma unroll
+      for (int o = 32; o > 0; o >>= 1) {
+#pragma unroll
+        for (int t = 0; t < 4; t++) v[t] += __shfl_xor(v[t], o, 64);
+      }
+      if (lane == 0) {
+#pragma unroll
+        for (int t = 0; t < 4; t++) zS[tid >> 6][t] = v[t];
+      }
+    }
+    __syncthreads();
+  }
+  if (tid < 4) {
+    int t = tid, tok = n0 + t;
+    float Z = zS[0][t] + zS[1][t] + zS[2][t] + zS[3][t];
+    float p1 = 1.f / Z;
+    float p2 = expf(m2[t] - m1[t]) / Z;
+    float s = p1 + p2 + EPSF;
+    int e1 = i1[t], e2 = i2[t];
+    int s1 = atomicAdd(&P.cnt[e1], 1); if (s1 > SLOTS - 1) s1 = SLOTS - 1;
+    int s2 = atomicAdd(&P.cnt[e2], 1); if (s2 > SLOTS - 1) s2 = SLOTS - 1;
+    int sl1 = e1 * SLOTS + s1, sl2 = e2 * SLOTS + s2;
+    P.slottok[sl1] = tok; P.slottok[sl2] = tok;
+    sE[t][0] = e1; sE[t][1] = e2;
+    sSlot[t][0] = sl1; sSlot[t][1] = sl2;
+    sWt[t][0] = p1 / s; sWt[t][1] = p2 / s;
+  }
+
+  __threadfence();
+  __syncthreads();
+  if (tid == 0) {
+    flag_add(&P.flags[FD_ROUTE]);
+    flag_wait(&P.flags[FD_ROUTE], 512);
+  }
+  __syncthreads();
+  __threadfence();
+
+  {
+    const int e = bid >> 1, sub = bid & 1;
+    int n = __hip_atomic_load(&P.cnt[e], __ATOMIC_RELAXED, __HIP_MEMORY_SCOPE_AGENT);
+    if (n > SLOTS) n = SLOTS;
+    const int base = e * SLOTS;
+    const float* Wp = P.expW + (size_t)e * Dd * Dd + j;
+    for (int t0 = sub * 16; t0 < n; t0 += 32) {
+      int m = n - t0; if (m > 16) m = 16;
+      __syncthreads();
+      for (int tt = g; tt < m; tt += 4) {
+        int tok = P.slottok[base + t0 + tt];
+        hT[j * 20 + tt] = P.h2buf[tok * Dd + j];
+      }
+      __syncthreads();
+      float acc[4] = {0, 0, 0, 0};
 #pragma unroll 8
-      for (int k = 0; k < 128; k++) acc += ob[k] * rot[k * 128 + tid];
-      bR[tid] = acc;
-    }
+      for (int i = 0; i < 128; i++) {
+        float w = Wp[i * Dd];
+        float4 h4 = *(const float4*)&hT[i * 20 + g * 4];
+        acc[0] += h4.x * w; acc[1] += h4.y * w; acc[2] += h4.z * w; acc[3] += h4.w * w;
+      }
+#pragma unroll
+      for (int k = 0; k < 4; k++) {
+        int tt = g * 4 + k;
+        if (tt < m) P.ybuf[(size_t)(base + t0 + tt) * Dd + j] = acc[k];
+      }
+    }
+    __threadfence();
+    __syncthreads();
+    if (tid == 0) flag_add(&P.flags[FD_EXP + e]);
+  }
+
+  if (tid < 8) {
+    int t = tid >> 1, sl = tid & 1;
+    flag_wait(&P.flags[FD_EXP + sE[t][sl]], 2);
+  }
+  __syncthreads();
+  __threadfence();
+
+  {
+    float y1 = P.ybuf[(size_t)sSlot[g][0] * Dd + j];
+    float y2 = P.ybuf[(size_t)sSlot[g][1] * Dd + j];
+    ((float*)&y1T[j])[g] = y1;
+    ((float*)&y2T[j])[g] = y2;
+    ((float*)&inT[j])[g] = sWt[g][0] * y1 + sWt[g][1] * y2;
+  }
+  __syncthreads();
+
+  {
+    float a0 = 0, a1 = 0, a2 = 0, a3 = 0;
+    const float* Wp = (g < 2 ? P.m1W : P.m2W) + ((g & 1) * 64) * Dd + j;
+#pragma unroll 16
+    for (int i = 0; i < 64; i++) {
+      float4 h4 = inT[(g & 1) * 64 + i];
+      float w = Wp[i * Dd];
+      a0 += h4.x * w; a1 += h4.y * w; a2 += h4.z * w; a3 += h4.w * w;
+    }
+    if (g) part[g - 1][j] = make_float4(a0, a1, a2, a3);
+    __syncthreads();
+    if (g == 0) {
+      float b1 = P.m1b[j], b2 = P.m2b[j];
+      float4 p0 = part[0][j], p1 = part[1][j], p2 = part[2][j];
+      float gv[4], uv[4];
+      gv[0] = a0 + p0.x + b1; gv[1] = a1 + p0.y + b1;
+      gv[2] = a2 + p0.z + b1; gv[3] = a3 + p0.w + b1;
+      uv[0] = p1.x + p2.x + b2; uv[1] = p1.y + p2.y + b2;
+      uv[2] = p1.z + p2.z + b2; uv[3] = p1.w + p2.w + b2;
+#pragma unroll
+      for (int t = 0; t < 4; t++) {
+        float sv = gv[t] * sigm(gv[t]) * uv[t];
+        ((float*)&sT[j])[t] = sv;
+        P.out[(n0 + t) * Dd + j] = xn[t] + sv;
+      }
+    }
+    __syncthreads();
+  }
+
+  if (tid < 128) {
+    float v[4];
+#pragma unroll
+    for (int t = 0; t < 4; t++) {
+      float sv = ((const float*)&sT[j])[t];
+      float d1 = ((const float*)&y1T[j])[t] - sv;
+      float d2 = ((const float*)&y2T[j])[t] - sv;
+      v[t] = sWt[t][0] * d1 * d1 + sWt[t][1] * d2 * d2;
+    }
+#pragma unroll
+    for (int o = 32; o > 0; o >>= 1) {
+#pragma unroll
+      for (int t = 0; t < 4; t++) v[t] += __shfl_xor(v[t], o, 64);
+    }
+    if (lane == 0) rtmp[tid >> 6] = make_float4(v[0], v[1], v[2], v[3]);
+  }
+  __syncthreads();
+  if (tid < 4) {
+    float s = ((const float*)&rtmp[0])[tid] + ((const float*)&rtmp[1])[tid];
+    P.out[NTOK * Dd + n0 + tid] = expf(-s * (1.f / 128.f));
   }
 }
 
-__global__ __launch_bounds__(512) void k_mid(
+__global__ __launch_bounds__(256) void k_ctx_fb(const float* __restrict__ kv,
+                                                float* __restrict__ ctx,
+                                                float* __restrict__ ksum) {
+  const int blk = blockIdx.x;
+  const int tid = threadIdx.x;
+  const int bh = blk >> 3, c = blk & 7;
+  const int b = bh >> 3, h = bh & 7;
+  const int d = tid >> 4, e = tid & 15;
+  __shared__ float sh[64 * 32];
+#pragma unroll
+  for (int r = 0; r < 8; r++) {
+    int lin = r * 256 + tid;
+    int tok = lin >> 5, off = lin & 31;
+    sh[lin] = kv[((b * TT + c * 64 + tok) * 256) + h * 32 + off];
+  }
+  __syncthreads();
+  float acc = 0.f, ks = 0.f;
+#pragma unroll 4
+  for (int t = 0; t < 64; t++) {
+    float kk = sh[t * 32 + d];
+    acc += kk * sh[t * 32 + 16 + e];
+    ks += kk;
+  }
+  atomicAdd(&ctx[bh * 256 + d * 16 + e], acc);
+  if (e == 0) atomicAdd(&ksum[bh * 16 + d], ks);
+}
+
+__global__ __launch_bounds__(512) void k_mid_fb(
     const float* __restrict__ x, const float* __restrict__ qbuf,
     const float* __restrict__ ctx, const float* __restrict__ ksum,
     const float* __restrict__ oR, const float* __restrict__ bR,
@@ -728,7 +617,7 @@
   const int tid = threadIdx.x;
   const int j = tid & 127, g = tid >> 7;
   const int lane = tid & 63;
-  const int n0 = blockIdx.x * TPBo;
+  const int n0 = blockIdx.x * 4;
   const int b = n0 >> 9;
 
   __shared__ float4 bufA[128], bufB[128];
@@ -743,7 +632,6 @@
 #pragma unroll
     for (int t = 0; t < 4; t++) xres[t] = x[(n0 + t) * Dd + j];
   }
-
   ((float*)&bufA[j])[g] = qbuf[(n0 + g) * Dd + j];
   __syncthreads();
 
@@ -979,20 +867,19 @@
   }
 }
 
-__global__ __launch_bounds__(512) void k_exp(const float* __restrict__ h2buf,
-                                             const int* __restrict__ slottok,
-                                             const int* __restrict__ cnt,
-                                             const float* __restrict__ expW,
-                                             float* __restrict__ ybuf) {
-  const int e = blockIdx.x;
+__global__ __launch_bounds__(512) void k_exp_fb(const float* __restrict__ h2buf,
+                                                const int* __restrict__ slottok,
+                                                const int* __restrict__ cnt,
+                                                const float* __restrict__ expW,
+                                                float* __restrict__ ybuf) {
+  const int e = blockIdx.x >> 1, sub = blockIdx.x & 1;
   int n = cnt[e]; if (n > SLOTS) n = SLOTS;
-  if (n == 0) return;
   const int base = e * SLOTS;
   const int tid = threadIdx.x;
   const int j = tid & 127, g = tid >> 7;
   __shared__ __align__(16) float hT[128 * 20];
   const float* Wp = expW + (size_t)e * Dd * Dd + j;
-  for (int t0 = 0; t0 < n; t0 += 16) {
+  for (int t0 = sub * 16; t0 < n; t0 += 32) {
     int m = n - t0; if (m > 16) m = 16;
     __syncthreads();
     for (int tt = g; tt < m; tt += 4) {
@@ -1015,7 +902,7 @@
   }
 }
 
-__global__ __launch_bounds__(512) void k_post(
+__global__ __launch_bounds__(512) void k_post_fb(
     const float* __restrict__ xnbuf, const float* __restrict__ ybuf,
     const int* __restrict__ tokslot, const float* __restrict__ gw,
     const float* __restrict__ m1W, const float* __restrict__ m1b,
@@ -1024,7 +911,7 @@
   const int tid = threadIdx.x;
   const int j = tid & 127, g = tid >> 7;
   const int lane = tid & 63;
-  const int n0 = blockIdx.x * TPBo;
+  const int n0 = blockIdx.x * 4;
 
   __shared__ float4 y1T[128], y2T[128], inT[128], sT[128];
   __shared__ float4 part[3][128];
@@ -1104,87 +991,76 @@
 extern "C" void kernel_launch(void* const* d_in, const int* in_sizes, int n_in,
                               void* d_out, int out_size, void* d_ws, size_t ws_size,
                               hipStream_t stream) {
-  float* ws = (float*)d_ws;
-
-  Params p;
-  p.x   = (const float*)d_in[0];
-  p.g1  = (const float*)d_in[1];
-  p.qW  = (const float*)d_in[2];
-  p.qb  = (const float*)d_in[3];
-  p.kdW = (const float*)d_in[4];
-  p.kdb = (const float*)d_in[5];
-  p.kuW = (const float*)d_in[6];
-  p.kub = (const float*)d_in[7];
-  p.oW  = (const float*)d_in[8];
-  p.ob  = (const float*)d_in[9];
-  p.rot = (const float*)d_in[10];
-  p.tqs = (const float*)d_in[11];
-  p.s1W = (const float*)d_in[12];
-  p.s1b = (const float*)d_in[13];
-  p.s2W = (const float*)d_in[14];
-  p.s2b = (const float*)d_in[15];
-  p.g2  = (const float*)d_in[16];
-  p.gateW = (const float*)d_in[17];
-  p.gateb = (const float*)d_in[18];
-  p.expW  = (const float*)d_in[19];
-  p.m1W = (const float*)d_in[20];
-  p.m1b = (const float*)d_in[21];
-  p.m2W = (const float*)d_in[22];
-  p.m2b = (const float*)d_in[23];
-  p.out = (float*)d_out;
-
-  p.ctx     = ws;
-  p.ksum    = ws + 8192;
-  p.oR      = ws + 8704;
-  p.bR      = ws + 25088;
-  p.h2buf   = ws + 25216;
-  p.cnt     = (int*)(ws + 287360);
-  p.slottok = (int*)(ws + 287616);
-  p.ybuf    = ws + 353152;
+  const float* x   = (const float*)d_in[0];
+  const float* g1  = (const float*)d_in[1];
+  const float* qW  = (const float*)d_in[2];
+  const float* qb  = (const float*)d_in[3];
+  const float* kdW = (const float*)d_in[4];
+  const float* kdb = (const float*)d_in[5];
+  const float* kuW = (const float*)d_in[6];
+  const float* kub = (const float*)d_in[7];
+  const float* oW  = (const float*)d_in[8];
+  const float* ob  = (const float*)d_in[9];
+  const float* rot = (const float*)d_in[10];
+  const float* tqs = (const float*)d_in[11];
+  const float* s1W = (const float*)d_in[12];
+  const float* s1b = (const float*)d_in[13];
+  const float* s2W = (const float*)d_in[14];
+  const float* s2b = (const float*)d_in[15];
+  const float* g2  = (const float*)d_in[16];
+  const float* gW  = (const float*)d_in[17];
+  const float* gb  = (const float*)d_in[18];
+  const float* eW  = (const float*)d_in[19];
+  const float* m1W = (const float*)d_in[20];
+  const float* m1b = (const float*)d_in[21];
+  const float* m2W = (const float*)d_in[22];
+  const float* m2b = (const float*)d_in[23];
+  float* out = (float*)d_out;
+  float* ws  = (float*)d_ws;
+
+  float* ctx     = ws;
+  float* ksum    = ws + 8192;
+  float* oR      = ws + 8704;
+  float* bR      = ws + 25088;
+  float* qbuf    = ws + 25216;
+  float* kvbuf   = ws + 287360;
+  float* h2buf   = ws + 811648;
+  float* ybuf    = ws + 1073792;
+  int*   cnt     = (int*)(ws + 9462400);
+  int*   slottok = (int*)(ws + 9462656);
+  int*   flags   = (int*)(ws + 9528192);
+  float* xnbuf   = ws + 9528576;
+  float* gw      = ws + 9790720;
+  int*   tokslot = (int*)(ws + 9794816);
+
+  k_pre<<<NTOK / 4, 512, 0, stream>>>(x, g1, qW, qb, kdW, kdb, kuW, kub,
+                                      oW, ob, rot, qbuf, kvbuf, ctx, ksum,
+                                      cnt, flags, oR, bR);
+
+  RParams p;
+  p.x = x; p.qbuf = qbuf; p.kvbuf = kvbuf; p.oR = oR; p.bR = bR; p.tqs = tqs;
+  p.s1W = s1W; p.s1b = s1b; p.s2W = s2W; p.s2b = s2b; p.g2 = g2;
+  p.gateW = gW; p.gateb = gb; p.expW = eW;
+  p.m1W = m1W; p.m1b = m1b; p.m2W = m2W; p.m2b = m2b;
+  p.ctx = ctx; p.ksum = ksum; p.h2buf = h2buf; p.ybuf = ybuf; p.out = out;
+  p.cnt = cnt; p.slottok = slottok; p.flags = flags;
 
   void* args[] = {(void*)&p};
   hipError_t err = hipErrorUnknown;
-
-  int nb4 = 0;
+  int nb = 0;
   if (hipOccupancyMaxActiveBlocksPerMultiprocessor(
-          &nb4, reinterpret_cast<const void*>(&k_fused4), 512, 0) != hipSuccess)
-    nb4 = 0;
-  if (nb4 >= 2) {
-    err = hipLaunchCooperativeKernel((void*)k_fused4, dim3(NTOK / 4), dim3(512),
+          &nb, reinterpret_cast<const void*>(&k_rest), 512, 0) == hipSuccess &&
+      nb >= 2) {
+    err = hipLaunchCooperativeKernel((void*)k_rest, dim3(NTOK / 4), dim3(512),
                                      args, 0u, stream);
   }
-  if (err != hipSuccess) {
-    int nb8 = 0;
-    if (hipOccupancyMaxActiveBlocksPerMultiprocessor(
-            &nb8, reinterpret_cast<const void*>(&k_fused8), 512, 0) == hipSuccess &&
-        nb8 >= 1) {
-      err = hipLaunchCooperativeKernel((void*)k_fused8, dim3(NTOK / 8), dim3(512),
-                                       args, 0u, stream);
-    }
-  }
   if (err == hipSuccess) return;
 
-  float* qbuf   = ws;
-  float* kvbuf  = ws + 262144;
-  float* ctx    = ws + 786432;
-  float* ksum   = ws + 794624;
-  float* h2buf  = ws + 795136;
-  float* xnbuf  = ws + 1057280;
-  float* gw     = ws + 1319424;
-  float* oRb    = ws + 1323520;
-  float* bRb    = ws + 1339904;
-  int*   cnt     = (int*)(ws + 1373056);
-  int*   tokslot = (int*)(ws + 1373312);
-  int*   slottok = (int*)(ws + 1377408);
-  float* ybuf   = ws + 1442944;
-
-  k_pre<<<NTOK / 4, 512, 0, stream>>>(p.x, p.g1, p.qW, p.qb, p.kdW, p.kdb, p.kuW, p.kub,
-                                      qbuf, kvbuf, ctx, ksum, cnt);
-  k_ctx<<<321, 256, 0, stream>>>(kvbuf, ctx, ksum, p.oW, p.ob, p.rot, oRb, bRb);
-  k_mid<<<NTOK / 4, 512, 0, stream>>>(p.x, qbuf, ctx, ksum, oRb, bRb, p.tqs,
-                                      p.s1W, p.s1b, p.s2W, p.s2b, p.g2, p.gateW, p.gateb,
-                                      xnbuf, h2buf, gw, tokslot, slottok, cnt);
-  k_exp<<<NE, 512, 0, stream>>>(h2buf, slottok, cnt, p.expW, ybuf);
-  k_post<<<NTOK / 4, 512, 0, stream>>>(xnbuf, ybuf, tokslot, gw,
-                                       p.m1W, p.m1b, p.m2W, p.m2b, p.out);
+  k_ctx_fb<<<256, 256, 0, stream>>>(kvbuf, ctx, ksum);
+  k_mid_fb<<<NTOK / 4, 512, 0, stream>>>(x, qbuf, ctx, ksum, oR, bR, tqs,
+                                         s1W, s1b, s2W, s2b, g2, gW, gb,
+                                         xnbuf, h2buf, gw, tokslot, slottok, cnt);
+  k_exp_fb<<<NE * 2, 512, 0, stream>>>(h2buf, slottok, cnt, eW, ybuf);
+  k_post_fb<<<NTOK / 4, 512, 0, stream>>>(xnbuf, ybuf, tokslot, gw,
+                                          m1W, m1b, m2W, m2b, out);
 }
```

After: 162.5 us. 2.4% less time.
